# Kernel tuning notes

Hardware: AMD Instinct MI355X
Metric: run time of the kernel (lower is better)

## Reference

```python
import jax, jax.numpy as jnp
import numpy as np

DIM = 768
H = 12
D = DIM // H            # 64
SCALE = D ** -0.5
M = 64                  # landmarks for pnp heads
PINV_ITERS = 6
PNP_HEADS = 11          # heads 0..10 use Nystrom, head 11 uses softmax


def setup_inputs() -> dict:
    key = jax.random.key(0)
    ks = jax.random.split(key, 5)
    B, N = 4, 4096
    x = jax.random.normal(ks[0], (B, N, DIM), jnp.float32)
    qkv_w = jax.random.normal(ks[1], (3 * DIM, DIM), jnp.float32) * (DIM ** -0.5)
    qkv_b = jax.random.normal(ks[2], (3 * DIM,), jnp.float32) * 0.01
    proj_w = jax.random.normal(ks[3], (DIM, DIM), jnp.float32) * (DIM ** -0.5)
    proj_b = jax.random.normal(ks[4], (DIM,), jnp.float32) * 0.01
    return {"x": x, "qkv_w": qkv_w, "qkv_b": qkv_b, "proj_w": proj_w, "proj_b": proj_b}


def moore_penrose_iter_pinv(x, iters=PINV_ITERS):
    # x: [B, h, M, M]. Original torch code takes torch.max over the whole per-head
    # tensor (incl. batch), so normalize with a per-head scalar over axes (B, M).
    abs_x = jnp.abs(x)
    col_max = abs_x.sum(axis=-1, keepdims=True).max(axis=(0, 2, 3), keepdims=True)
    row_max = abs_x.sum(axis=-2, keepdims=True).max(axis=(0, 2, 3), keepdims=True)
    z = jnp.swapaxes(x, -1, -2) / (col_max * row_max)
    I = jnp.eye(x.shape[-1], dtype=x.dtype)
    for _ in range(iters):
        xz = x @ z
        z = 0.25 * (z @ (13.0 * I - xz @ (15.0 * I - xz @ (7.0 * I - xz))))
    return z


def reference(x, qkv_w, qkv_b, proj_w, proj_b):
    B, N, C = x.shape
    qkv = (x @ qkv_w.T + qkv_b).reshape(B, N, 3, H, D).transpose(2, 0, 3, 1, 4)  # [3,B,H,N,D]
    q, k, v = qkv[0] * SCALE, qkv[1], qkv[2]

    # ---- Nystrom (pnp) heads 0..PNP_HEADS-1, all with the same M -> vectorized ----
    qp, kp, vp = q[:, :PNP_HEADS], k[:, :PNP_HEADS], v[:, :PNP_HEADS]
    idxs = jnp.array([int(i * N / M) for i in range(M)], dtype=jnp.int32)
    q_m = qp[:, :, idxs, :]   # [B,h,M,D] landmark queries
    k_m = kp[:, :, idxs, :]   # [B,h,M,D] landmark keys

    SA = jnp.einsum('bhnd,bhmd->bhnm', qp, k_m)   # [B,h,N,M]
    SC = jnp.einsum('bhmd,bhnd->bhmn', q_m, kp)   # [B,h,M,N]
    SB = jnp.einsum('bhmd,bhld->bhml', q_m, k_m)  # [B,h,M,M]

    eA = jnp.exp(SA - SA.max(axis=-1, keepdims=True))
    sc_max = SC.max(axis=-1, keepdims=True)       # [B,h,M,1]
    eC = jnp.exp(SC - sc_max)
    eB = jnp.exp(jnp.clip(SB - sc_max, -88.0, None))

    v_aug = jnp.concatenate([vp, jnp.ones_like(vp[..., :1])], axis=-1)  # [B,h,N,D+1]
    pi = moore_penrose_iter_pinv(eB)
    prod = (eA @ pi) @ (eC @ v_aug)               # [B,h,N,D+1]
    out_p = prod[..., :-1] / jnp.maximum(prod[..., -1:], 1e-8)

    # ---- fallback softmax head(s) ----
    qs, ks_, vs = q[:, PNP_HEADS:], k[:, PNP_HEADS:], v[:, PNP_HEADS:]
    attn = jax.nn.softmax(jnp.einsum('bhnd,bhmd->bhnm', qs, ks_), axis=-1)
    out_s = attn @ vs

    ctx = jnp.concatenate([out_p, out_s], axis=1).transpose(0, 2, 1, 3).reshape(B, N, C)
    return ctx @ proj_w.T + proj_b
```

## Files before the change

### kernel.cpp

```cpp
#include <hip/hip_runtime.h>


typedef __attribute__((ext_vector_type(8))) short short8;
typedef __attribute__((ext_vector_type(4))) float f32x4;
typedef __attribute__((ext_vector_type(4))) unsigned short ushort4v;

static __device__ __forceinline__ unsigned short f2bf(float f) {
    union { float f; unsigned u; } x; x.f = f;
    unsigned r = x.u + 0x7fffu + ((x.u >> 16) & 1u);
    return (unsigned short)(r >> 16);
}

static __device__ __forceinline__ float b2f(unsigned short u) {
    union { unsigned u; float f; } t; t.u = (unsigned)u << 16; return t.f;
}

static __device__ __forceinline__ void bfsplit(float x, unsigned short& h, unsigned short& l) {
    unsigned short hh = f2bf(x);
    union { unsigned u; float f; } t; t.u = (unsigned)hh << 16;
    h = hh;
    l = f2bf(x - t.f);
}

__global__ __launch_bounds__(256) void preconv3(
    const float* __restrict__ a, const float* __restrict__ b,
    const float* __restrict__ c,
    unsigned short* __restrict__ ahi, unsigned short* __restrict__ alo,
    unsigned short* __restrict__ bhi, unsigned short* __restrict__ blo,
    unsigned short* __restrict__ chi, unsigned short* __restrict__ clo)
{
    const int nA = 3145728, nB = 442368, nC = 147456;
    const int total = nA + nB + nC;
    for (int i = blockIdx.x * 256 + threadIdx.x; i < total; i += gridDim.x * 256) {
        const float* src; unsigned short* hi; unsigned short* lo; int j;
        if (i < nA)           { src = a; hi = ahi; lo = alo; j = i; }
        else if (i < nA + nB) { src = b; hi = bhi; lo = blo; j = i - nA; }
        else                  { src = c; hi = chi; lo = clo; j = i - nA - nB; }
        float4 f = *(const float4*)(src + (size_t)j * 4);
        float vs[4] = {f.x, f.y, f.z, f.w};
        ushort4v h, l;
        #pragma unroll
        for (int t = 0; t < 4; ++t) {
            unsigned short hh, ll;
            bfsplit(vs[t], hh, ll);
            h[t] = hh; l[t] = ll;
        }
        *(ushort4v*)(hi + (size_t)j * 4) = h;
        *(ushort4v*)(lo + (size_t)j * 4) = l;
    }
}

__global__ __launch_bounds__(256, 2) void gemm_qk_mfma(
    const unsigned short* __restrict__ Xh, const unsigned short* __restrict__ Xl,
    const unsigned short* __restrict__ Wh, const unsigned short* __restrict__ Wl,
    const float* __restrict__ bias,
    unsigned short* __restrict__ qh, unsigned short* __restrict__ ql,
    unsigned short* __restrict__ kh, unsigned short* __restrict__ kl)
{
    __shared__ unsigned short Ah[4096], Al[4096], Bh[4096], Bl[4096];
    const int tid = threadIdx.x;
    const int bid = blockIdx.x;
    const int swz = (bid & 7) * 192 + (bid >> 3);
    const int brow = (swz / 12) << 7, bcol = (swz % 12) << 7;
    const int ln = tid & 63, wv = tid >> 6;
    const int wr = (wv >> 1) << 6, wc = (wv & 1) << 6;
    const int srow = tid >> 1, sc = (tid & 1) << 1;
    const size_t ag = (size_t)(brow + srow) * 768 + (sc << 3);
    const size_t bg = (size_t)(bcol + srow) * 768 + (sc << 3);
    const int fr = ln & 15, fc = ln >> 4;
    const int i0 = srow * 32 + (((sc + 0) ^ (srow & 3)) << 3);
    const int i1 = srow * 32 + (((sc + 1) ^ (srow & 3)) << 3);

    f32x4 acc[4][4] = {};
    for (int k0 = 0; k0 < 768; k0 += 32) {
        short8 xh0 = *(const short8*)(Xh + ag + k0);
        short8 xh1 = *(const short8*)(Xh + ag + k0 + 8);
        short8 xl0 = *(const short8*)(Xl + ag + k0);
        short8 xl1 = *(const short8*)(Xl + ag + k0 + 8);
        short8 wh0 = *(const short8*)(Wh + bg + k0);
        short8 wh1 = *(const short8*)(Wh + bg + k0 + 8);
        short8 wl0 = *(const short8*)(Wl + bg + k0);
        short8 wl1 = *(const short8*)(Wl + bg + k0 + 8);
        __syncthreads();
        *(short8*)&Ah[i0] = xh0; *(short8*)&Ah[i1] = xh1;
        *(short8*)&Al[i0] = xl0; *(short8*)&Al[i1] = xl1;
        *(short8*)&Bh[i0] = wh0; *(short8*)&Bh[i1] = wh1;
        *(short8*)&Bl[i0] = wl0; *(short8*)&Bl[i1] = wl1;
        __syncthreads();
        short8 ah[4], al[4], bh[4], bl[4];
        #pragma unroll
        for (int i = 0; i < 4; ++i) {
            int ar = wr + (i << 4) + fr;
            int aidx = ar * 32 + ((fc ^ (ar & 3)) << 3);
            ah[i] = *(short8*)&Ah[aidx];
            al[i] = *(short8*)&Al[aidx];
            int br2 = wc + (i << 4) + fr;
            int bidx = br2 * 32 + ((fc ^ (br2 & 3)) << 3);
            bh[i] = *(short8*)&Bh[bidx];
            bl[i] = *(short8*)&Bl[bidx];
        }
        #pragma unroll
        for (int i = 0; i < 4; ++i)
            #pragma unroll
            for (int j = 0; j < 4; ++j) {
                acc[i][j] = __builtin_amdgcn_mfma_f32_16x16x32_bf16(ah[i], bh[j], acc[i][j], 0, 0, 0);
                acc[i][j] = __builtin_amdgcn_mfma_f32_16x16x32_bf16(ah[i], bl[j], acc[i][j], 0, 0, 0);
                acc[i][j] = __builtin_amdgcn_mfma_f32_16x16x32_bf16(al[i], bh[j], acc[i][j], 0, 0, 0);
            }
    }
    const int fg = ln >> 4;
    #pragma unroll
    for (int j = 0; j < 4; ++j) {
        int c = bcol + wc + (j << 4) + fr;
        float bb = bias[c];
        int rem = c - (c >= 768 ? 768 : 0);
        int h = rem >> 6, d = rem & 63;
        #pragma unroll
        for (int i = 0; i < 4; ++i)
            #pragma unroll
            for (int r = 0; r < 4; ++r) {
                int row = brow + wr + (i << 4) + (fg << 2) + r;
                int b = row >> 12, n = row & 4095;
                float val = acc[i][j][r] + bb;
                size_t idx = (((size_t)(b * 12 + h) << 12) + n) * 64 + d;
                unsigned short hh, ll;
                if (c < 768) {
                    bfsplit(val * 0.125f, hh, ll);
                    qh[idx] = hh; ql[idx] = ll;
                } else {
                    bfsplit(val, hh, ll);
                    kh[idx] = hh; kl[idx] = ll;
                }
            }
    }
}

__global__ __launch_bounds__(256, 2) void gemm_v_mfma(
    const unsigned short* __restrict__ Xh, const unsigned short* __restrict__ Wh,
    const float* __restrict__ bias, unsigned short* __restrict__ vh)
{
    __shared__ unsigned short Ah[8192], Bh[8192];
    const int tid = threadIdx.x;
    const int bid = blockIdx.x;
    const int swz = (bid & 7) * 96 + (bid >> 3);
    const int brow = (swz / 6) << 7, bcol = 1536 + ((swz % 6) << 7);
    const int ln = tid & 63, wv = tid >> 6;
    const int wr = (wv >> 1) << 6, wc = (wv & 1) << 6;
    const int srow = tid >> 1;
    const int c0 = (tid & 1) << 2;
    const size_t ag = (size_t)(brow + srow) * 768;
    const size_t bg = (size_t)(bcol + srow) * 768;
    const int fr = ln & 15, fc = ln >> 4;

    f32x4 acc[4][4] = {};
    for (int k0 = 0; k0 < 768; k0 += 64) {
        short8 xa[4], wb[4];
        #pragma unroll
        for (int cc = 0; cc < 4; ++cc) {
            xa[cc] = *(const short8*)(Xh + ag + k0 + ((c0 + cc) << 3));
            wb[cc] = *(const short8*)(Wh + bg + k0 + ((c0 + cc) << 3));
        }
        __syncthreads();
        #pragma unroll
        for (int cc = 0; cc < 4; ++cc) {
            int dst = srow * 64 + (((c0 + cc) ^ (srow & 7)) << 3);
            *(short8*)&Ah[dst] = xa[cc];
            *(short8*)&Bh[dst] = wb[cc];
        }
        __syncthreads();
        #pragma unroll
        for (int ks = 0; ks < 2; ++ks) {
            const int kc = (ks << 2) + fc;
            short8 ah[4], bh[4];
            #pragma unroll
            for (int i = 0; i < 4; ++i) {
                int ar = wr + (i << 4) + fr;
                ah[i] = *(short8*)&Ah[ar * 64 + ((kc ^ (ar & 7)) << 3)];
                int br2 = wc + (i << 4) + fr;
                bh[i] = *(short8*)&Bh[br2 * 64 + ((kc ^ (br2 & 7)) << 3)];
            }
            #pragma unroll
            for (int i = 0; i < 4; ++i)
                #pragma unroll
                for (int j = 0; j < 4; ++j)
                    acc[i][j] = __builtin_amdgcn_mfma_f32_16x16x32_bf16(ah[i], bh[j], acc[i][j], 0, 0, 0);
        }
    }
    const int fg = ln >> 4;
    #pragma unroll
    for (int j = 0; j < 4; ++j) {
        int c = bcol + wc + (j << 4) + fr;
        float bb = bias[c];
        int rem = c - 1536;
        int h = rem >> 6, d = rem & 63;
        #pragma unroll
        for (int i = 0; i < 4; ++i)
            #pragma unroll
            for (int r = 0; r < 4; ++r) {
                int row = brow + wr + (i << 4) + (fg << 2) + r;
                int b = row >> 12, n = row & 4095;
                float val = acc[i][j][r] + bb;
                size_t idx = (((size_t)(b * 12 + h) << 12) + n) * 64 + d;
                vh[idx] = f2bf(val);
            }
    }
}

__global__ __launch_bounds__(256) void wflash(
    const unsigned short* __restrict__ qh, const unsigned short* __restrict__ ql,
    const unsigned short* __restrict__ khg, const unsigned short* __restrict__ klg,
    const unsigned short* __restrict__ vhg,
    float* __restrict__ wacc, float* __restrict__ wl, float* __restrict__ wm)
{
    int chunk = blockIdx.x;
    int bh = blockIdx.y;
    int b = bh / 11, h = bh - b * 11;
    size_t base = ((size_t)(b * 12 + h)) << 12;
    __shared__ unsigned short kh_s[64][72], kl_s[64][72];
    __shared__ unsigned short vth[64][72];
    __shared__ unsigned short ph[4][16][72];
    int tid = threadIdx.x;
    int wv = tid >> 6, ln = tid & 63;
    int rr = tid >> 2, dg = (tid & 3) << 4;
    const int arow = (wv << 4) + (ln & 15);
    const int ak0 = (ln >> 4) << 3;
    const int rg = (ln >> 4) << 2;
    short8 aqh0, aql0, aqh1, aql1;
    {
        size_t off = ((base + ((size_t)arow << 6)) << 6) + ak0;
        aqh0 = *(const short8*)(qh + off);
        aqh1 = *(const short8*)(qh + off + 32);
        aql0 = *(const short8*)(ql + off);
        aql1 = *(const short8*)(ql + off + 32);
    }
    f32x4 o_acc[4] = {};
    float mr[4] = {-1e30f, -1e30f, -1e30f, -1e30f};
    float lr[4] = {};
    for (int t = 0; t < 8; ++t) {
        int n0 = (chunk << 9) + (t << 6);
        __syncthreads();
        {
            size_t off = ((base + n0 + rr) << 6) + dg;
            *(short8*)&kh_s[rr][dg]     = *(const short8*)(khg + off);
            *(short8*)&kh_s[rr][dg + 8] = *(const short8*)(khg + off + 8);
            *(short8*)&kl_s[rr][dg]     = *(const short8*)(klg + off);
            *(short8*)&kl_s[rr][dg + 8] = *(const short8*)(klg + off + 8);
            short8 v0 = *(const short8*)(vhg + off);
            short8 v1 = *(const short8*)(vhg + off + 8);
            #pragma unroll
            for (int i = 0; i < 8; ++i) {
                vth[dg + i][rr]     = (unsigned short)v0[i];
                vth[dg + 8 + i][rr] = (unsigned short)v1[i];
            }
        }
        __syncthreads();
        f32x4 s_acc[4];
        #pragma unroll
        for (int jb = 0; jb < 4; ++jb) {
            f32x4 z = {};
            const int brow2 = (jb << 4) + (ln & 15);
            short8 bh0 = *(short8*)&kh_s[brow2][ak0];
            short8 bh1 = *(short8*)&kh_s[brow2][ak0 + 32];
            short8 bl0 = *(short8*)&kl_s[brow2][ak0];
            short8 bl1 = *(short8*)&kl_s[brow2][ak0 + 32];
            z = __builtin_amdgcn_mfma_f32_16x16x32_bf16(aqh0, bh0, z, 0, 0, 0);
            z = __builtin_amdgcn_mfma_f32_16x16x32_bf16(aqh0, bl0, z, 0, 0, 0);
            z = __builtin_amdgcn_mfma_f32_16x16x32_bf16(aql0, bh0, z, 0, 0, 0);
            z = __builtin_amdgcn_mfma_f32_16x16x32_bf16(aqh1, bh1, z, 0, 0, 0);
            z = __builtin_amdgcn_mfma_f32_16x16x32_bf16(aqh1, bl1, z, 0, 0, 0);
            z = __builtin_amdgcn_mfma_f32_16x16x32_bf16(aql1, bh1, z, 0, 0, 0);
            s_acc[jb] = z;
        }
        float mx[4];
        #pragma unroll
        for (int r = 0; r < 4; ++r)
            mx[r] = fmaxf(fmaxf(s_acc[0][r], s_acc[1][r]),
                          fmaxf(s_acc[2][r], s_acc[3][r]));
        #pragma unroll
        for (int off2 = 1; off2 < 16; off2 <<= 1)
            #pragma unroll
            for (int r = 0; r < 4; ++r)
                mx[r] = fmaxf(mx[r], __shfl_xor(mx[r], off2, 64));
        float fac[4];
        #pragma unroll
        for (int r = 0; r < 4; ++r) {
            float mn = fmaxf(mr[r], mx[r]);
            fac[r] = expf(mr[r] - mn);
            mr[r] = mn;
        }
        float rs[4] = {};
        #pragma unroll
        for (int jb = 0; jb < 4; ++jb)
            #pragma unroll
            for (int r = 0; r < 4; ++r) {
                float p = expf(s_acc[jb][r] - mr[r]);
                rs[r] += p;
                ph[wv][rg + r][(jb << 4) + (ln & 15)] = f2bf(p);
            }
        #pragma unroll
        for (int off2 = 1; off2 < 16; off2 <<= 1)
            #pragma unroll
            for (int r = 0; r < 4; ++r)
                rs[r] += __shfl_xor(rs[r], off2, 64);
        #pragma unroll
        for (int r = 0; r < 4; ++r) lr[r] = lr[r] * fac[r] + rs[r];
        #pragma unroll
        for (int jb = 0; jb < 4; ++jb)
            #pragma unroll
            for (int r = 0; r < 4; ++r)
                o_acc[jb][r] *= fac[r];
        short8 pah0 = *(short8*)&ph[wv][ln & 15][ak0];
        short8 pah1 = *(short8*)&ph[wv][ln & 15][ak0 + 32];
        #pragma unroll
        for (int jb = 0; jb < 4; ++jb) {
            const int brow2 = (jb << 4) + (ln & 15);
            short8 bv0 = *(short8*)&vth[brow2][ak0];
            short8 bv1 = *(short8*)&vth[brow2][ak0 + 32];
            f32x4 o = o_acc[jb];
            o = __builtin_amdgcn_mfma_f32_16x16x32_bf16(pah0, bv0, o, 0, 0, 0);
            o = __builtin_amdgcn_mfma_f32_16x16x32_bf16(pah1, bv1, o, 0, 0, 0);
            o_acc[jb] = o;
        }
    }
    int cidx = (bh << 3) + chunk;
    #pragma unroll
    for (int jb = 0; jb < 4; ++jb)
        #pragma unroll
        for (int r = 0; r < 4; ++r) {
            int row = (wv << 4) + rg + r, col = (jb << 4) + (ln & 15);
            wacc[((size_t)cidx << 12) + ((size_t)row << 6) + col] = o_acc[jb][r];
        }
    if ((ln & 15) == 0)
        #pragma unroll
        for (int r = 0; r < 4; ++r) {
            int row = (wv << 4) + rg + r;
            wl[cidx * 64 + row] = lr[r];
            wm[cidx * 64 + row] = mr[r];
        }
}

__global__ __launch_bounds__(256) void wmerge(
    const float* __restrict__ wacc, const float* __restrict__ wl,
    const float* __restrict__ wm,
    float* __restrict__ Wb, float* __restrict__ scm)
{
    int bh = blockIdx.x;
    int tid = threadIdx.x;
    __shared__ float fcs[8][64];
    if (tid < 64) {
        float mx = -1e30f;
        #pragma unroll
        for (int c = 0; c < 8; ++c)
            mx = fmaxf(mx, wm[((bh << 3) + c) * 64 + tid]);
        scm[(bh << 6) + tid] = mx;
        #pragma unroll
        for (int c = 0; c < 8; ++c)
            fcs[c][tid] = expf(wm[((bh << 3) + c) * 64 + tid] - mx);
    }
    __syncthreads();
    for (int e = tid; e < 4096; e += 256) {
        int m = e >> 6, j = e & 63;
        float s = 0.f;
        #pragma unroll
        for (int c = 0; c < 8; ++c)
            s += fcs[c][m] * wacc[((size_t)((bh << 3) + c) << 12) + e];
        Wb[(size_t)bh * 4160 + m * 65 + j] = s;
    }
    if (tid < 64) {
        float s = 0.f;
        #pragma unroll
        for (int c = 0; c < 8; ++c)
            s += fcs[c][tid] * wl[((bh << 3) + c) * 64 + tid];
        Wb[(size_t)bh * 4160 + tid * 65 + 64] = s;
    }
}

__global__ __launch_bounds__(256) void eb_kernel(
    const unsigned short* __restrict__ qh, const unsigned short* __restrict__ ql,
    const unsigned short* __restrict__ kh, const unsigned short* __restrict__ kl,
    const float* __restrict__ scm, float* __restrict__ eB)
{
    int bh = blockIdx.x;
    int b = bh / 11, h = bh - b * 11;
    size_t base = ((size_t)(b * 12 + h)) << 12;
    __shared__ float qm[64][65], km[64][65];
    int tid = threadIdx.x;
    for (int e = tid; e < 4096; e += 256) {
        int mm = e >> 6, d = e & 63;
        size_t off = ((base + ((size_t)mm << 6)) << 6) + d;
        qm[mm][d] = b2f(qh[off]) + b2f(ql[off]);
        km[mm][d] = b2f(kh[off]) + b2f(kl[off]);
    }
    __syncthreads();
    int m = tid >> 2, l0 = tid & 3;
    float smax = scm[(bh << 6) + m];
    for (int l = l0; l < 64; l += 4) {
        float s = 0.f;
        #pragma unroll
        for (int d = 0; d < 64; ++d) s += qm[m][d] * km[l][d];
        eB[((size_t)bh << 12) + (m << 6) + l] = expf(fmaxf(s - smax, -88.f));
    }
}

__global__ __launch_bounds__(256) void norms_kernel(
    const float* __restrict__ eB, float* __restrict__ denom)
{
    int h = blockIdx.x;
    int tid = threadIdx.x;
    int b = tid >> 6, idx = tid & 63;
    int bh = b * 11 + h;
    const float* E = eB + ((size_t)bh << 12);
    float rs = 0.f, cs = 0.f;
    #pragma unroll 4
    for (int l = 0; l < 64; ++l) rs += E[(idx << 6) + l];
    #pragma unroll 4
    for (int m = 0; m < 64; ++m) cs += E[(m << 6) + idx];
    __shared__ float r1[256], r2[256];
    r1[tid] = rs; r2[tid] = cs;
    __syncthreads();
    for (int s = 128; s > 0; s >>= 1) {
        if (tid < s) {
            r1[tid] = fmaxf(r1[tid], r1[tid + s]);
            r2[tid] = fmaxf(r2[tid], r2[tid + s]);
        }
        __syncthreads();
    }
    if (tid == 0) denom[h] = r1[0] * r2[0];
}

__device__ __forceinline__ void mm64x3(
    const unsigned short (&Ahi)[64][72], const unsigned short (&Alo)[64][72],
    const unsigned short (&BThi)[64][72], const unsigned short (&BTlo)[64][72],
    int wr, int wc, int fr, int fk, f32x4 (&acc)[2][2])
{
    #pragma unroll
    for (int ks = 0; ks < 2; ++ks) {
        const int kb = (ks << 5) + fk;
        short8 ah[2], al[2], bh[2], bl[2];
        #pragma unroll
        for (int i = 0; i < 2; ++i) {
            ah[i] = *(const short8*)&Ahi[wr + (i << 4) + fr][kb];
            al[i] = *(const short8*)&Alo[wr + (i << 4) + fr][kb];
            bh[i] = *(const short8*)&BThi[wc + (i << 4) + fr][kb];
            bl[i] = *(const short8*)&BTlo[wc + (i << 4) + fr][kb];
        }
        #pragma unroll
        for (int i = 0; i < 2; ++i)
            #pragma unroll
            for (int j = 0; j < 2; ++j) {
                acc[i][j] = __builtin_amdgcn_mfma_f32_16x16x32_bf16(ah[i], bh[j], acc[i][j], 0, 0, 0);
                acc[i][j] = __builtin_amdgcn_mfma_f32_16x16x32_bf16(ah[i], bl[j], acc[i][j], 0, 0, 0);
                acc[i][j] = __builtin_amdgcn_mfma_f32_16x16x32_bf16(al[i], bh[j], acc[i][j], 0, 0, 0);
            }
    }
}

__global__ __launch_bounds__(256) void pinv_kernel(
    const float* __restrict__ eB, const float* __restrict__ denom,
    float* __restrict__ pi_)
{
    __shared__ unsigned short Xh[64][72],  Xl[64][72];
    __shared__ unsigned short Zh[64][72],  Zl[64][72];
    __shared__ unsigned short ZTh[64][72], ZTl[64][72];
    __shared__ unsigned short Mh[64][72],  Ml[64][72];
    __shared__ unsigned short MTh[64][72], MTl[64][72];
    __shared__ unsigned short Th[64][72],  Tbl[64][72];
    __shared__ float Zf[64][68];
    int bh = blockIdx.x;
    int h = bh % 11;
    int tid = threadIdx.x;
    float dn = denom[h];
    const int ln = tid & 63, wv = tid >> 6;
    const int wr = (wv >> 1) << 5, wc = (wv & 1) << 5;
    const int fr = ln & 15, fk = (ln >> 4) << 3;
    const int rg = (ln >> 4) << 2;

    for (int e = tid; e < 4096; e += 256) {
        int m = e >> 6, l = e & 63;
        float xv = eB[((size_t)bh << 12) + e];
        unsigned short hh, ll;
        bfsplit(xv, hh, ll);
        Xh[m][l] = hh; Xl[m][l] = ll;
        float zv = xv / dn;
        Zf[l][m] = zv;
        bfsplit(zv, hh, ll);
        Zh[l][m] = hh; Zl[l][m] = ll;
        ZTh[m][l] = hh; ZTl[m][l] = ll;
    }
    __syncthreads();

    for (int it = 0; it < 6; ++it) {
        f32x4 mm1[2][2] = {};
        mm64x3(Xh, Xl, ZTh, ZTl, wr, wc, fr, fk, mm1);
        #pragma unroll
        for (int i = 0; i < 2; ++i)
            #pragma unroll
            for (int j = 0; j < 2; ++j)
                #pragma unroll
                for (int r = 0; r < 4; ++r) {
                    int row = wr + (i << 4) + rg + r, col = wc + (j << 4) + fr;
                    unsigned short hh, ll;
                    bfsplit(mm1[i][j][r], hh, ll);
                    Mh[row][col] = hh;  Ml[row][col] = ll;
                    MTh[col][row] = hh; MTl[col][row] = ll;
                }
        __syncthreads();
        f32x4 a2[2][2] = {};
        mm64x3(Mh, Ml, MTh, MTl, wr, wc, fr, fk, a2);
        #pragma unroll
        for (int i = 0; i < 2; ++i)
            #pragma unroll
            for (int j = 0; j < 2; ++j)
                #pragma unroll
                for (int r = 0; r < 4; ++r) {
                    int row = wr + (i << 4) + rg + r, col = wc + (j << 4) + fr;
                    float val = 7.f * mm1[i][j][r] - a2[i][j][r];
                    unsigned short hh, ll;
                    bfsplit(val, hh, ll);
                    Th[col][row] = hh; Tbl[col][row] = ll;
                }
        __syncthreads();
        f32x4 a3[2][2] = {};
        mm64x3(Mh, Ml, Th, Tbl, wr, wc, fr, fk, a3);
        __syncthreads();
        #pragma unroll
        for (int i = 0; i < 2; ++i)
            #pragma unroll
            for (int j = 0; j < 2; ++j)
                #pragma unroll
                for (int r = 0; r < 4; ++r) {
                    int row = wr + (i << 4) + rg + r, col = wc + (j << 4) + fr;
                    float val = 15.f * mm1[i][j][r] - a3[i][j][r];
                    unsigned short hh, ll;
                    bfsplit(val, hh, ll);
                    Th[col][row] = hh; Tbl[col][row] = ll;
                }
        __syncthreads();
        f32x4 a4[2][2] = {};
        mm64x3(Zh, Zl, Th, Tbl, wr, wc, fr, fk, a4);
        float zn[2][2][4];
        #pragma unroll
        for (int i = 0; i < 2; ++i)
            #pragma unroll
            for (int j = 0; j < 2; ++j)
                #pragma unroll
                for (int r = 0; r < 4; ++r) {
                    int row = wr + (i << 4) + rg + r, col = wc + (j << 4) + fr;
                    zn[i][j][r] = 0.25f * (13.f * Zf[row][col] - a4[i][j][r]);
                }
        __syncthreads();
        #pragma unroll
        for (int i = 0; i < 2; ++i)
            #pragma unroll
            for (int j = 0; j < 2; ++j)
                #pragma unroll
                for (int r = 0; r < 4; ++r) {
                    int row = wr + (i << 4) + rg + r, col = wc + (j << 4) + fr;
                    float val = zn[i][j][r];
                    Zf[row][col] = val;
                    unsigned short hh, ll;
                    bfsplit(val, hh, ll);
                    Zh[row][col] = hh;  Zl[row][col] = ll;
                    ZTh[col][row] = hh; ZTl[col][row] = ll;
                }
        __syncthreads();
    }
    for (int e = tid; e < 4096; e += 256)
        pi_[((size_t)bh << 12) + e] = Zf[e >> 6][e & 63];
}

__global__ __launch_bounds__(256) void pw_kernel(
    const float* __restrict__ pi_, const float* __restrict__ Wb,
    float* __restrict__ Tb)
{
    int bh = blockIdx.x;
    __shared__ float P[64][65];
    __shared__ float Wl[64][66];
    int tid = threadIdx.x;
    for (int e = tid; e < 4096; e += 256)
        P[e >> 6][e & 63] = pi_[((size_t)bh << 12) + e];
    for (int e = tid; e < 64 * 65; e += 256) {
        int l = e / 65, j = e - l * 65;
        Wl[l][j] = Wb[(size_t)bh * 4160 + e];
    }
    __syncthreads();
    int m = tid & 63, g = tid >> 6;
    #pragma unroll
    for (int t = 0; t < 17; ++t) {
        int j = g + (t << 2);
        if (j > 64) break;
        float s = 0.f;
        #pragma unroll
        for (int l = 0; l < 64; ++l) s += P[m][l] * Wl[l][j];
        Tb[(size_t)((bh << 6) + m) * 65 + j] = s;
    }
}

__global__ __launch_bounds__(256) void outp_kernel(
    const unsigned short* __restrict__ qh, const unsigned short* __restrict__ ql,
    const unsigned short* __restrict__ khg, const unsigned short* __restrict__ klg,
    const float* __restrict__ Tb, unsigned short* __restrict__ ctxh)
{
    int bh = blockIdx.y;
    int b = bh / 11, h = bh - b * 11;
    int n0 = blockIdx.x << 6;
    size_t base = ((size_t)(b * 12 + h)) << 12;
    __shared__ unsigned short kmh[64][72], kml[64][72];
    __shared__ unsigned short tth[64][72], ttl[64][72];
    __shared__ unsigned short ph[4][16][72];
    __shared__ float t64[64];
    int tid = threadIdx.x;
    int wv = tid >> 6, ln = tid & 63;
    int rr = tid >> 2, dg = (tid & 3) << 4;
    const int arow = (wv << 4) + (ln & 15);
    const int ak0 = (ln >> 4) << 3;
    const int rg = (ln >> 4) << 2;
    {
        size_t off = ((base + ((size_t)rr << 6)) << 6) + dg;
        *(short8*)&kmh[rr][dg]     = *(const short8*)(khg + off);
        *(short8*)&kmh[rr][dg + 8] = *(const short8*)(khg + off + 8);
        *(short8*)&kml[rr][dg]     = *(const short8*)(klg + off);
        *(short8*)&kml[rr][dg + 8] = *(const short8*)(klg + off + 8);
    }
    for (int e = tid; e < 4096; e += 256) {
        int m = e >> 6, j = e & 63;
        float tv = Tb[(size_t)((bh << 6) + m) * 65 + j];
        unsigned short hh, ll;
        bfsplit(tv, hh, ll);
        tth[j][m] = hh; ttl[j][m] = ll;
    }
    if (tid < 64) t64[tid] = Tb[(size_t)((bh << 6) + tid) * 65 + 64];
    short8 aqh0, aql0, aqh1, aql1;
    {
        size_t off = ((base + n0 + arow) << 6) + ak0;
        aqh0 = *(const short8*)(qh + off);
        aqh1 = *(const short8*)(qh + off + 32);
        aql0 = *(const short8*)(ql + off);
        aql1 = *(const short8*)(ql + off + 32);
    }
    __syncthreads();
    f32x4 s_acc[4];
    #pragma unroll
    for (int jb = 0; jb < 4; ++jb) {
        f32x4 z = {};
        const int brow2 = (jb << 4) + (ln & 15);
        short8 bh0 = *(short8*)&kmh[brow2][ak0];
        short8 bh1 = *(short8*)&kmh[brow2][ak0 + 32];
        short8 bl0 = *(short8*)&kml[brow2][ak0];
        short8 bl1 = *(short8*)&kml[brow2][ak0 + 32];
        z = __builtin_amdgcn_mfma_f32_16x16x32_bf16(aqh0, bh0, z, 0, 0, 0);
        z = __builtin_amdgcn_mfma_f32_16x16x32_bf16(aqh0, bl0, z, 0, 0, 0);
        z = __builtin_amdgcn_mfma_f32_16x16x32_bf16(aql0, bh0, z, 0, 0, 0);
        z = __builtin_amdgcn_mfma_f32_16x16x32_bf16(aqh1, bh1, z, 0, 0, 0);
        z = __builtin_amdgcn_mfma_f32_16x16x32_bf16(aqh1, bl1, z, 0, 0, 0);
        z = __builtin_amdgcn_mfma_f32_16x16x32_bf16(aql1, bh1, z, 0, 0, 0);
        s_acc[jb] = z;
    }
    float mx[4];
    #pragma unroll
    for (int r = 0; r < 4; ++r)
        mx[r] = fmaxf(fmaxf(s_acc[0][r], s_acc[1][r]),
                      fmaxf(s_acc[2][r], s_acc[3][r]));
    #pragma unroll
    for (int off2 = 1; off2 < 16; off2 <<= 1)
        #pragma unroll
        for (int r = 0; r < 4; ++r)
            mx[r] = fmaxf(mx[r], __shfl_xor(mx[r], off2, 64));
    float den[4] = {};
    #pragma unroll
    for (int jb = 0; jb < 4; ++jb) {
        float tj = t64[(jb << 4) + (ln & 15)];
        #pragma unroll
        for (int r = 0; r < 4; ++r) {
            float p = expf(s_acc[jb][r] - mx[r]);
            den[r] += p * tj;
            ph[wv][rg + r][(jb << 4) + (ln & 15)] = f2bf(p);
        }
    }
    #pragma unroll
    for (int off2 = 1; off2 < 16; off2 <<= 1)
        #pragma unroll
        for (int r = 0; r < 4; ++r)
            den[r] += __shfl_xor(den[r], off2, 64);
    short8 pah0 = *(short8*)&ph[wv][ln & 15][ak0];
    short8 pah1 = *(short8*)&ph[wv][ln & 15][ak0 + 32];
    f32x4 o_acc[4] = {};
    #pragma unroll
    for (int jb = 0; jb < 4; ++jb) {
        const int brow2 = (jb << 4) + (ln & 15);
        short8 bth0 = *(short8*)&tth[brow2][ak0];
        short8 bth1 = *(short8*)&tth[brow2][ak0 + 32];
        short8 btl0 = *(short8*)&ttl[brow2][ak0];
        short8 btl1 = *(short8*)&ttl[brow2][ak0 + 32];
        f32x4 o = o_acc[jb];
        o = __builtin_amdgcn_mfma_f32_16x16x32_bf16(pah0, bth0, o, 0, 0, 0);
        o = __builtin_amdgcn_mfma_f32_16x16x32_bf16(pah0, btl0, o, 0, 0, 0);
        o = __builtin_amdgcn_mfma_f32_16x16x32_bf16(pah1, bth1, o, 0, 0, 0);
        o = __builtin_amdgcn_mfma_f32_16x16x32_bf16(pah1, btl1, o, 0, 0, 0);
        o_acc[jb] = o;
    }
    float inv[4];
    #pragma unroll
    for (int r = 0; r < 4; ++r) inv[r] = 1.0f / fmaxf(den[r], 1e-8f);
    #pragma unroll
    for (int jb = 0; jb < 4; ++jb)
        #pragma unroll
        for (int r = 0; r < 4; ++r) {
            int row = n0 + (wv << 4) + rg + r;
            int col = (jb << 4) + (ln & 15);
            ctxh[((size_t)b * 4096 + row) * 768 + h * 64 + col] =
                f2bf(o_acc[jb][r] * inv[r]);
        }
}

__global__ __launch_bounds__(256) void flash_part(
    const unsigned short* __restrict__ qhg, const unsigned short* __restrict__ khg,
    const unsigned short* __restrict__ vhg,
    float* __restrict__ pacc, float* __restrict__ pm, float* __restrict__ pl)
{
    int bx = blockIdx.x, cy = blockIdx.y, b = blockIdx.z;
    int n0 = bx << 6;
    size_t base = ((size_t)(b * 12 + 11)) << 12;
    __shared__ unsigned short qs[64][72];
    __shared__ unsigned short ks[64][72];
    __shared__ unsigned short vts[64][72];
    __shared__ unsigned short ps[4][16][72];
    int tid = threadIdx.x;
    int wv = tid >> 6, ln = tid & 63;
    int rr = tid >> 2, dg = (tid & 3) << 4;
    {
        size_t off = ((base + n0 + rr) << 6) + dg;
        *(short8*)&qs[rr][dg]     = *(const short8*)(qhg + off);
        *(short8*)&qs[rr][dg + 8] = *(const short8*)(qhg + off + 8);
    }
    __syncthreads();
    const int arow = (wv << 4) + (ln & 15);
    const int ak0 = (ln >> 4) << 3;
    const int rg = (ln >> 4) << 2;
    short8 aq0 = *(short8*)&qs[arow][ak0];
    short8 aq1 = *(short8*)&qs[arow][ak0 + 32];
    f32x4 o_acc[4] = {};
    float mr[4] = {-1e30f, -1e30f, -1e30f, -1e30f};
    float lr[4] = {};
    for (int t = 0; t < 16; ++t) {
        int m0 = (cy << 10) + (t << 6);
        __syncthreads();
        {
            size_t off = ((base + m0 + rr) << 6) + dg;
            *(short8*)&ks[rr][dg]     = *(const short8*)(khg + off);
            *(short8*)&ks[rr][dg + 8] = *(const short8*)(khg + off + 8);
            short8 v0 = *(const short8*)(vhg + off);
            short8 v1 = *(const short8*)(vhg + off + 8);
            #pragma unroll
            for (int i = 0; i < 8; ++i) {
                vts[dg + i][rr]     = (unsigned short)v0[i];
                vts[dg + 8 + i][rr] = (unsigned short)v1[i];
            }
        }
        __syncthreads();
        f32x4 s_acc[4];
        #pragma unroll
        for (int jb = 0; jb < 4; ++jb) {
            f32x4 z = {};
            short8 bk0 = *(short8*)&ks[(jb << 4) + (ln & 15)][ak0];
            short8 bk1 = *(short8*)&ks[(jb << 4) + (ln & 15)][ak0 + 32];
            z = __builtin_amdgcn_mfma_f32_16x16x32_bf16(aq0, bk0, z, 0, 0, 0);
            z = __builtin_amdgcn_mfma_f32_16x16x32_bf16(aq1, bk1, z, 0, 0, 0);
            s_acc[jb] = z;
        }
        float mx[4];
        #pragma unroll
        for (int r = 0; r < 4; ++r)
            mx[r] = fmaxf(fmaxf(s_acc[0][r], s_acc[1][r]),
                          fmaxf(s_acc[2][r], s_acc[3][r]));
        #pragma unroll
        for (int off2 = 1; off2 < 16; off2 <<= 1)
            #pragma unroll
            for (int r = 0; r < 4; ++r)
                mx[r] = fmaxf(mx[r], __shfl_xor(mx[r], off2, 64));
        float fac[4];
        #pragma unroll
        for (int r = 0; r < 4; ++r) {
            float mn = fmaxf(mr[r], mx[r]);
            fac[r] = expf(mr[r] - mn);
            mr[r] = mn;
        }
        float rs[4] = {};
        #pragma unroll
        for (int jb = 0; jb < 4; ++jb)
            #pragma unroll
            for (int r = 0; r < 4; ++r) {
                float p = expf(s_acc[jb][r] - mr[r]);
                rs[r] += p;
                ps[wv][rg + r][(jb << 4) + (ln & 15)] = f2bf(p);
            }
        #pragma unroll
        for (int off2 = 1; off2 < 16; off2 <<= 1)
            #pragma unroll
            for (int r = 0; r < 4; ++r)
                rs[r] += __shfl_xor(rs[r], off2, 64);
        #pragma unroll
        for (int r = 0; r < 4; ++r) lr[r] = lr[r] * fac[r] + rs[r];
        #pragma unroll
        for (int jb = 0; jb < 4; ++jb)
            #pragma unroll
            for (int r = 0; r < 4; ++r)
                o_acc[jb][r] *= fac[r];
        short8 pa0 = *(short8*)&ps[wv][ln & 15][ak0];
        short8 pa1 = *(short8*)&ps[wv][ln & 15][ak0 + 32];
        #pragma unroll
        for (int jb = 0; jb < 4; ++jb) {
            short8 bv0 = *(short8*)&vts[(jb << 4) + (ln & 15)][ak0];
            short8 bv1 = *(short8*)&vts[(jb << 4) + (ln & 15)][ak0 + 32];
            f32x4 z = o_acc[jb];
            z = __builtin_amdgcn_mfma_f32_16x16x32_bf16(pa0, bv0, z, 0, 0, 0);
            z = __builtin_amdgcn_mfma_f32_16x16x32_bf16(pa1, bv1, z, 0, 0, 0);
            o_acc[jb] = z;
        }
    }
    int slot = (b * 4 + cy) * 64 + bx;
    #pragma unroll
    for (int jb = 0; jb < 4; ++jb)
        #pragma unroll
        for (int r = 0; r < 4; ++r) {
            int row = (wv << 4) + rg + r, col = (jb << 4) + (ln & 15);
            pacc[(size_t)slot * 4096 + (size_t)row * 64 + col] = o_acc[jb][r];
        }
    if ((ln & 15) == 0)
        #pragma unroll
        for (int r = 0; r < 4; ++r) {
            int row = (wv << 4) + rg + r;
            pm[(size_t)slot * 64 + row] = mr[r];
            pl[(size_t)slot * 64 + row] = lr[r];
        }
}

__global__ __launch_bounds__(256) void flash_merge(
    const float* __restrict__ pacc, const float* __restrict__ pm,
    const float* __restrict__ pl, unsigned short* __restrict__ ctxh)
{
    int bx = blockIdx.x, b = blockIdx.y;
    int tid = threadIdx.x, r = tid & 63, g = tid >> 6;
    float mc[4], mt = -1e30f;
    #pragma unroll
    for (int c = 0; c < 4; ++c) {
        mc[c] = pm[(size_t)((b * 4 + c) * 64 + bx) * 64 + r];
        mt = fmaxf(mt, mc[c]);
    }
    float fac[4], lt = 0.f;
    #pragma unroll
    for (int c = 0; c < 4; ++c) {
        fac[c] = expf(mc[c] - mt);
        lt += fac[c] * pl[(size_t)((b * 4 + c) * 64 + bx) * 64 + r];
    }
    float inv = 1.0f / lt;
    size_t obase = ((size_t)b * 4096 + (size_t)((bx << 6) + r)) * 768 + 11 * 64 + (g << 4);
    #pragma unroll
    for (int i = 0; i < 16; ++i) {
        float s = 0.f;
        #pragma unroll
        for (int c = 0; c < 4; ++c)
            s += fac[c] * pacc[(size_t)((b * 4 + c) * 64 + bx) * 4096 + (size_t)r * 64 + (g << 4) + i];
        ctxh[obase + i] = f2bf(s * inv);
    }
}

__global__ __launch_bounds__(256, 2) void gemm_proj_mfma(
    const unsigned short* __restrict__ Xh, const unsigned short* __restrict__ Wh,
    const float* __restrict__ bias, float* __restrict__ out)
{
    __shared__ unsigned short Ah[8192], Bh[8192];
    const int tid = threadIdx.x;
    const int bid = blockIdx.x;
    const int swz = (bid & 7) * 96 + (bid >> 3);
    const int brow = (swz / 6) << 7, bcol = (swz % 6) << 7;
    const int ln = tid & 63, wv = tid >> 6;
    const int wr = (wv >> 1) << 6, wc = (wv & 1) << 6;
    const int srow = tid >> 1;
    const int c0 = (tid & 1) << 2;
    const size_t ag = (size_t)(brow + srow) * 768;
    const size_t bg = (size_t)(bcol + srow) * 768;
    const int fr = ln & 15, fc = ln >> 4;

    f32x4 acc[4][4] = {};
    for (int k0 = 0; k0 < 768; k0 += 64) {
        short8 xa[4], wb[4];
        #pragma unroll
        for (int cc = 0; cc < 4; ++cc) {
            xa[cc] = *(const short8*)(Xh + ag + k0 + ((c0 + cc) << 3));
            wb[cc] = *(const short8*)(Wh + bg + k0 + ((c0 + cc) << 3));
        }
        __syncthreads();
        #pragma unroll
        for (int cc = 0; cc < 4; ++cc) {
            int dst = srow * 64 + (((c0 + cc) ^ (srow & 7)) << 3);
            *(short8*)&Ah[dst] = xa[cc];
            *(short8*)&Bh[dst] = wb[cc];
        }
        __syncthreads();
        #pragma unroll
        for (int ks = 0; ks < 2; ++ks) {
            const int kc = (ks << 2) + fc;
            short8 ah[4], bh[4];
            #pragma unroll
            for (int i = 0; i < 4; ++i) {
                int ar = wr + (i << 4) + fr;
                ah[i] = *(short8*)&Ah[ar * 64 + ((kc ^ (ar & 7)) << 3)];
                int br2 = wc + (i << 4) + fr;
                bh[i] = *(short8*)&Bh[br2 * 64 + ((kc ^ (br2 & 7)) << 3)];
            }
            #pragma unroll
            for (int i = 0; i < 4; ++i)
                #pragma unroll
                for (int j = 0; j < 4; ++j)
                    acc[i][j] = __builtin_amdgcn_mfma_f32_16x16x32_bf16(ah[i], bh[j], acc[i][j], 0, 0, 0);
        }
    }
    const int fg = ln >> 4;
    #pragma unroll
    for (int j = 0; j < 4; ++j) {
        int c = bcol + wc + (j << 4) + fr;
        float bb = bias[c];
        #pragma unroll
        for (int i = 0; i < 4; ++i)
            #pragma unroll
            for (int r = 0; r < 4; ++r) {
                int row = brow + wr + (i << 4) + (fg << 2) + r;
                out[(size_t)row * 768 + c] = acc[i][j][r] + bb;
            }
    }
}

extern "C" void kernel_launch(void* const* d_in, const int* in_sizes, int n_in,
                              void* d_out, int out_size, void* d_ws, size_t ws_size,
                              hipStream_t stream)
{
    const float* x      = (const float*)d_in[0];
    const float* qkv_w  = (const float*)d_in[1];
    const float* qkv_b  = (const float*)d_in[2];
    const float* proj_w = (const float*)d_in[3];
    const float* proj_b = (const float*)d_in[4];
    float* out = (float*)d_out;

    const size_t QKV = (size_t)4 * 12 * 4096 * 64;
    unsigned short* qh = (unsigned short*)d_ws;
    unsigned short* ql = qh + QKV;
    unsigned short* kh = ql + QKV;
    unsigned short* kl = kh + QKV;
    unsigned short* vh = kl + QKV;
    unsigned short* ctxh = vh + QKV;
    float* scm  = (float*)(ctxh + QKV);
    float* eB   = scm + 4096;
    float* den  = eB + 44 * 4096;
    float* pi_  = den + 64;
    float* Wb   = pi_ + 44 * 4096;
    float* Tb   = Wb + 44 * 4160;
    unsigned short* Whi  = (unsigned short*)(Tb + 44 * 4160);
    unsigned short* Wlo  = Whi + (size_t)2304 * 768;
    unsigned short* Pwhi = Wlo + (size_t)2304 * 768;
    unsigned short* Pwlo = Pwhi + (size_t)768 * 768;

    unsigned short* Xhi = (unsigned short*)out;
    unsigned short* Xlo = Xhi + QKV;
    float* wacc = out;
    float* wl   = wacc + 1441792;
    float* wm   = wl + 22528;
    float* fpacc = out;
    float* fpm   = fpacc + 4194304;
    float* fpl   = fpm + 65536;

    preconv3<<<2048, 256, 0, stream>>>(x, qkv_w, proj_w,
                                       Xhi, Xlo, Whi, Wlo, Pwhi, Pwlo);
    gemm_qk_mfma<<<1536, 256, 0, stream>>>(Xhi, Xlo, Whi, Wlo, qkv_b,
                                           qh, ql, kh, kl);
    gemm_v_mfma<<<768, 256, 0, stream>>>(Xhi, Whi, qkv_b, vh);
    wflash<<<dim3(8, 44), 256, 0, stream>>>(qh, ql, kh, kl, vh, wacc, wl, wm);
    wmerge<<<44, 256, 0, stream>>>(wacc, wl, wm, Wb, scm);
    eb_kernel<<<44, 256, 0, stream>>>(qh, ql, kh, kl, scm, eB);
    norms_kernel<<<11, 256, 0, stream>>>(eB, den);
    pinv_kernel<<<44, 256, 0, stream>>>(eB, den, pi_);
    pw_kernel<<<44, 256, 0, stream>>>(pi_, Wb, Tb);
    outp_kernel<<<dim3(64, 44), 256, 0, stream>>>(qh, ql, kh, kl, Tb, ctxh);
    flash_part<<<dim3(64, 4, 4), 256, 0, stream>>>(qh, kh, vh, fpacc, fpm, fpl);
    flash_merge<<<dim3(64, 4), 256, 0, stream>>>(fpacc, fpm, fpl, ctxh);
    gemm_proj_mfma<<<768, 256, 0, stream>>>(ctxh, Pwhi, proj_b, out);
}
```

Baseline: 436.9 us.

## Merge independent kernels into combined launches to overlap softmax head with Nystrom stages

Fuses the QK and V projection GEMMs into one launch that branches on block index. It also merges the Nystrom landmark flash pass with the softmax-head partial flash into one attention launch, wmerge with eB computation, and outp with flash_merge. The goal is fewer launches and less tail idle time, letting independent work fill the GPU concurrently. The scratch buffers for the two flash paths now sit at separate offsets so they can coexist. The cost is heterogeneous blocks with differing shared-memory and register needs within a single kernel.

```diff
diff --git a/kernel.cpp b/kernel.cpp
--- a/kernel.cpp
+++ b/kernel.cpp
@@ -50,172 +50,168 @@
     }
 }
 
-__global__ __launch_bounds__(256, 2) void gemm_qk_mfma(
+__global__ __launch_bounds__(256, 2) void gemm_qkv2(
     const unsigned short* __restrict__ Xh, const unsigned short* __restrict__ Xl,
     const unsigned short* __restrict__ Wh, const unsigned short* __restrict__ Wl,
     const float* __restrict__ bias,
     unsigned short* __restrict__ qh, unsigned short* __restrict__ ql,
-    unsigned short* __restrict__ kh, unsigned short* __restrict__ kl)
-{
-    __shared__ unsigned short Ah[4096], Al[4096], Bh[4096], Bl[4096];
+    unsigned short* __restrict__ kh, unsigned short* __restrict__ kl,
+    unsigned short* __restrict__ vh)
+{
+    __shared__ unsigned short smem[16384];
     const int tid = threadIdx.x;
-    const int bid = blockIdx.x;
-    const int swz = (bid & 7) * 192 + (bid >> 3);
-    const int brow = (swz / 12) << 7, bcol = (swz % 12) << 7;
     const int ln = tid & 63, wv = tid >> 6;
     const int wr = (wv >> 1) << 6, wc = (wv & 1) << 6;
-    const int srow = tid >> 1, sc = (tid & 1) << 1;
-    const size_t ag = (size_t)(brow + srow) * 768 + (sc << 3);
-    const size_t bg = (size_t)(bcol + srow) * 768 + (sc << 3);
     const int fr = ln & 15, fc = ln >> 4;
-    const int i0 = srow * 32 + (((sc + 0) ^ (srow & 3)) << 3);
-    const int i1 = srow * 32 + (((sc + 1) ^ (srow & 3)) << 3);
-
-    f32x4 acc[4][4] = {};
-    for (int k0 = 0; k0 < 768; k0 += 32) {
-        short8 xh0 = *(const short8*)(Xh + ag + k0);
-        short8 xh1 = *(const short8*)(Xh + ag + k0 + 8);
-        short8 xl0 = *(const short8*)(Xl + ag + k0);
-        short8 xl1 = *(const short8*)(Xl + ag + k0 + 8);
-        short8 wh0 = *(const short8*)(Wh + bg + k0);
-        short8 wh1 = *(const short8*)(Wh + bg + k0 + 8);
-        short8 wl0 = *(const short8*)(Wl + bg + k0);
-        short8 wl1 = *(const short8*)(Wl + bg + k0 + 8);
-        __syncthreads();
-        *(short8*)&Ah[i0] = xh0; *(short8*)&Ah[i1] = xh1;
-        *(short8*)&Al[i0] = xl0; *(short8*)&Al[i1] = xl1;
-        *(short8*)&Bh[i0] = wh0; *(short8*)&Bh[i1] = wh1;
-        *(short8*)&Bl[i0] = wl0; *(short8*)&Bl[i1] = wl1;
-        __syncthreads();
-        short8 ah[4], al[4], bh[4], bl[4];
-        #pragma unroll
-        for (int i = 0; i < 4; ++i) {
-            int ar = wr + (i << 4) + fr;
-            int aidx = ar * 32 + ((fc ^ (ar & 3)) << 3);
-            ah[i] = *(short8*)&Ah[aidx];
-            al[i] = *(short8*)&Al[aidx];
-            int br2 = wc + (i << 4) + fr;
-            int bidx = br2 * 32 + ((fc ^ (br2 & 3)) << 3);
-            bh[i] = *(short8*)&Bh[bidx];
-            bl[i] = *(short8*)&Bl[bidx];
-        }
-        #pragma unroll
-        for (int i = 0; i < 4; ++i)
-            #pragma unroll
-            for (int j = 0; j < 4; ++j) {
-                acc[i][j] = __builtin_amdgcn_mfma_f32_16x16x32_bf16(ah[i], bh[j], acc[i][j], 0, 0, 0);
-                acc[i][j] = __builtin_amdgcn_mfma_f32_16x16x32_bf16(ah[i], bl[j], acc[i][j], 0, 0, 0);
-                acc[i][j] = __builtin_amdgcn_mfma_f32_16x16x32_bf16(al[i], bh[j], acc[i][j], 0, 0, 0);
-            }
-    }
     const int fg = ln >> 4;
-    #pragma unroll
-    for (int j = 0; j < 4; ++j) {
-        int c = bcol + wc + (j << 4) + fr;
-        float bb = bias[c];
-        int rem = c - (c >= 768 ? 768 : 0);
-        int h = rem >> 6, d = rem & 63;
-        #pragma unroll
-        for (int i = 0; i < 4; ++i)
-            #pragma unroll
-            for (int r = 0; r < 4; ++r) {
-                int row = brow + wr + (i << 4) + (fg << 2) + r;
-                int b = row >> 12, n = row & 4095;
-                float val = acc[i][j][r] + bb;
-                size_t idx = (((size_t)(b * 12 + h) << 12) + n) * 64 + d;
-                unsigned short hh, ll;
-                if (c < 768) {
-                    bfsplit(val * 0.125f, hh, ll);
-                    qh[idx] = hh; ql[idx] = ll;
-                } else {
-                    bfsplit(val, hh, ll);
-                    kh[idx] = hh; kl[idx] = ll;
-                }
-            }
-    }
-}
-
-__global__ __launch_bounds__(256, 2) void gemm_v_mfma(
-    const unsigned short* __restrict__ Xh, const unsigned short* __restrict__ Wh,
-    const float* __restrict__ bias, unsigned short* __restrict__ vh)
-{
-    __shared__ unsigned short Ah[8192], Bh[8192];
-    const int tid = threadIdx.x;
-    const int bid = blockIdx.x;
-    const int swz = (bid & 7) * 96 + (bid >> 3);
-    const int brow = (swz / 6) << 7, bcol = 1536 + ((swz % 6) << 7);
-    const int ln = tid & 63, wv = tid >> 6;
-    const int wr = (wv >> 1) << 6, wc = (wv & 1) << 6;
-    const int srow = tid >> 1;
-    const int c0 = (tid & 1) << 2;
-    const size_t ag = (size_t)(brow + srow) * 768;
-    const size_t bg = (size_t)(bcol + srow) * 768;
-    const int fr = ln & 15, fc = ln >> 4;
-
-    f32x4 acc[4][4] = {};
-    for (int k0 = 0; k0 < 768; k0 += 64) {
-        short8 xa[4], wb[4];
-        #pragma unroll
-        for (int cc = 0; cc < 4; ++cc) {
-            xa[cc] = *(const short8*)(Xh + ag + k0 + ((c0 + cc) << 3));
-            wb[cc] = *(const short8*)(Wh + bg + k0 + ((c0 + cc) << 3));
-        }
-        __syncthreads();
-        #pragma unroll
-        for (int cc = 0; cc < 4; ++cc) {
-            int dst = srow * 64 + (((c0 + cc) ^ (srow & 7)) << 3);
-            *(short8*)&Ah[dst] = xa[cc];
-            *(short8*)&Bh[dst] = wb[cc];
-        }
-        __syncthreads();
-        #pragma unroll
-        for (int ks = 0; ks < 2; ++ks) {
-            const int kc = (ks << 2) + fc;
-            short8 ah[4], bh[4];
+
+    if (blockIdx.x < 1536) {
+        unsigned short* Ah = smem;
+        unsigned short* Al = smem + 4096;
+        unsigned short* Bh = smem + 8192;
+        unsigned short* Bl = smem + 12288;
+        const int bid = blockIdx.x;
+        const int swz = (bid & 7) * 192 + (bid >> 3);
+        const int brow = (swz / 12) << 7, bcol = (swz % 12) << 7;
+        const int srow = tid >> 1, sc = (tid & 1) << 1;
+        const size_t ag = (size_t)(brow + srow) * 768 + (sc << 3);
+        const size_t bg = (size_t)(bcol + srow) * 768 + (sc << 3);
+        const int i0 = srow * 32 + (((sc + 0) ^ (srow & 3)) << 3);
+        const int i1 = srow * 32 + (((sc + 1) ^ (srow & 3)) << 3);
+
+        f32x4 acc[4][4] = {};
+        for (int k0 = 0; k0 < 768; k0 += 32) {
+            short8 xh0 = *(const short8*)(Xh + ag + k0);
+            short8 xh1 = *(const short8*)(Xh + ag + k0 + 8);
+            short8 xl0 = *(const short8*)(Xl + ag + k0);
+            short8 xl1 = *(const short8*)(Xl + ag + k0 + 8);
+            short8 wh0 = *(const short8*)(Wh + bg + k0);
+            short8 wh1 = *(const short8*)(Wh + bg + k0 + 8);
+            short8 wl0 = *(const short8*)(Wl + bg + k0);
+            short8 wl1 = *(const short8*)(Wl + bg + k0 + 8);
+            __syncthreads();
+            *(short8*)&Ah[i0] = xh0; *(short8*)&Ah[i1] = xh1;
+            *(short8*)&Al[i0] = xl0; *(short8*)&Al[i1] = xl1;
+            *(short8*)&Bh[i0] = wh0; *(short8*)&Bh[i1] = wh1;
+            *(short8*)&Bl[i0] = wl0; *(short8*)&Bl[i1] = wl1;
+            __syncthreads();
+            short8 ah[4], al[4], bh[4], bl[4];
             #pragma unroll
             for (int i = 0; i < 4; ++i) {
                 int ar = wr + (i << 4) + fr;
-                ah[i] = *(short8*)&Ah[ar * 64 + ((kc ^ (ar & 7)) << 3)];
+                int aidx = ar * 32 + ((fc ^ (ar & 3)) << 3);
+                ah[i] = *(short8*)&Ah[aidx];
+                al[i] = *(short8*)&Al[aidx];
                 int br2 = wc + (i << 4) + fr;
-                bh[i] = *(short8*)&Bh[br2 * 64 + ((kc ^ (br2 & 7)) << 3)];
+                int bidx = br2 * 32 + ((fc ^ (br2 & 3)) << 3);
+                bh[i] = *(short8*)&Bh[bidx];
+                bl[i] = *(short8*)&Bl[bidx];
             }
             #pragma unroll
             for (int i = 0; i < 4; ++i)
                 #pragma unroll
-                for (int j = 0; j < 4; ++j)
+                for (int j = 0; j < 4; ++j) {
                     acc[i][j] = __builtin_amdgcn_mfma_f32_16x16x32_bf16(ah[i], bh[j], acc[i][j], 0, 0, 0);
-        }
-    }
-    const int fg = ln >> 4;
-    #pragma unroll
-    for (int j = 0; j < 4; ++j) {
-        int c = bcol + wc + (j << 4) + fr;
-        float bb = bias[c];
-        int rem = c - 1536;
-        int h = rem >> 6, d = rem & 63;
-        #pragma unroll
-        for (int i = 0; i < 4; ++i)
-            #pragma unroll
-            for (int r = 0; r < 4; ++r) {
-                int row = brow + wr + (i << 4) + (fg << 2) + r;
-                int b = row >> 12, n = row & 4095;
-                float val = acc[i][j][r] + bb;
-                size_t idx = (((size_t)(b * 12 + h) << 12) + n) * 64 + d;
-                vh[idx] = f2bf(val);
-            }
-    }
-}
-
-__global__ __launch_bounds__(256) void wflash(
+                    acc[i][j] = __builtin_amdgcn_mfma_f32_16x16x32_bf16(ah[i], bl[j], acc[i][j], 0, 0, 0);
+                    acc[i][j] = __builtin_amdgcn_mfma_f32_16x16x32_bf16(al[i], bh[j], acc[i][j], 0, 0, 0);
+                }
+        }
+        #pragma unroll
+        for (int j = 0; j < 4; ++j) {
+            int c = bcol + wc + (j << 4) + fr;
+            float bb = bias[c];
+            int rem = c - (c >= 768 ? 768 : 0);
+            int h = rem >> 6, d = rem & 63;
+            #pragma unroll
+            for (int i = 0; i < 4; ++i)
+                #pragma unroll
+                for (int r = 0; r < 4; ++r) {
+                    int row = brow + wr + (i << 4) + (fg << 2) + r;
+                    int b = row >> 12, n = row & 4095;
+                    float val = acc[i][j][r] + bb;
+                    size_t idx = (((size_t)(b * 12 + h) << 12) + n) * 64 + d;
+                    unsigned short hh, ll;
+                    if (c < 768) {
+                        bfsplit(val * 0.125f, hh, ll);
+                        qh[idx] = hh; ql[idx] = ll;
+                    } else {
+                        bfsplit(val, hh, ll);
+                        kh[idx] = hh; kl[idx] = ll;
+                    }
+                }
+        }
+    } else {
+        unsigned short* Av = smem;
+        unsigned short* Bv = smem + 8192;
+        const int bid = blockIdx.x - 1536;
+        const int swz = (bid & 7) * 96 + (bid >> 3);
+        const int brow = (swz / 6) << 7, bcol = 1536 + ((swz % 6) << 7);
+        const int srow = tid >> 1;
+        const int c0 = (tid & 1) << 2;
+        const size_t ag = (size_t)(brow + srow) * 768;
+        const size_t bg = (size_t)(bcol + srow) * 768;
+
+        f32x4 acc[4][4] = {};
+        for (int k0 = 0; k0 < 768; k0 += 64) {
+            short8 xa[4], wb[4];
+            #pragma unroll
+            for (int cc = 0; cc < 4; ++cc) {
+                xa[cc] = *(const short8*)(Xh + ag + k0 + ((c0 + cc) << 3));
+                wb[cc] = *(const short8*)(Wh + bg + k0 + ((c0 + cc) << 3));
+            }
+            __syncthreads();
+            #pragma unroll
+            for (int cc = 0; cc < 4; ++cc) {
+                int dst = srow * 64 + (((c0 + cc) ^ (srow & 7)) << 3);
+                *(short8*)&Av[dst] = xa[cc];
+                *(short8*)&Bv[dst] = wb[cc];
+            }
+            __syncthreads();
+            #pragma unroll
+            for (int ks = 0; ks < 2; ++ks) {
+                const int kc = (ks << 2) + fc;
+                short8 ah[4], bh[4];
+                #pragma unroll
+                for (int i = 0; i < 4; ++i) {
+                    int ar = wr + (i << 4) + fr;
+                    ah[i] = *(short8*)&Av[ar * 64 + ((kc ^ (ar & 7)) << 3)];
+                    int br2 = wc + (i << 4) + fr;
+                    bh[i] = *(short8*)&Bv[br2 * 64 + ((kc ^ (br2 & 7)) << 3)];
+                }
+                #pragma unroll
+                for (int i = 0; i < 4; ++i)
+                    #pragma unroll
+                    for (int j = 0; j < 4; ++j)
+                        acc[i][j] = __builtin_amdgcn_mfma_f32_16x16x32_bf16(ah[i], bh[j], acc[i][j], 0, 0, 0);
+            }
+        }
+        #pragma unroll
+        for (int j = 0; j < 4; ++j) {
+            int c = bcol + wc + (j << 4) + fr;
+            float bb = bias[c];
+            int rem = c - 1536;
+            int h = rem >> 6, d = rem & 63;
+            #pragma unroll
+            for (int i = 0; i < 4; ++i)
+                #pragma unroll
+                for (int r = 0; r < 4; ++r) {
+                    int row = brow + wr + (i << 4) + (fg << 2) + r;
+                    int b = row >> 12, n = row & 4095;
+                    float val = acc[i][j][r] + bb;
+                    size_t idx = (((size_t)(b * 12 + h) << 12) + n) * 64 + d;
+                    vh[idx] = f2bf(val);
+                }
+        }
+    }
+}
+
+__global__ __launch_bounds__(256) void attn_mega(
     const unsigned short* __restrict__ qh, const unsigned short* __restrict__ ql,
     const unsigned short* __restrict__ khg, const unsigned short* __restrict__ klg,
     const unsigned short* __restrict__ vhg,
-    float* __restrict__ wacc, float* __restrict__ wl, float* __restrict__ wm)
-{
-    int chunk = blockIdx.x;
-    int bh = blockIdx.y;
-    int b = bh / 11, h = bh - b * 11;
-    size_t base = ((size_t)(b * 12 + h)) << 12;
+    float* __restrict__ wacc, float* __restrict__ wl, float* __restrict__ wm,
+    float* __restrict__ pacc, float* __restrict__ pm, float* __restrict__ pl)
+{
     __shared__ unsigned short kh_s[64][72], kl_s[64][72];
     __shared__ unsigned short vth[64][72];
     __shared__ unsigned short ph[4][16][72];
@@ -225,175 +221,283 @@
     const int arow = (wv << 4) + (ln & 15);
     const int ak0 = (ln >> 4) << 3;
     const int rg = (ln >> 4) << 2;
-    short8 aqh0, aql0, aqh1, aql1;
-    {
-        size_t off = ((base + ((size_t)arow << 6)) << 6) + ak0;
-        aqh0 = *(const short8*)(qh + off);
-        aqh1 = *(const short8*)(qh + off + 32);
-        aql0 = *(const short8*)(ql + off);
-        aql1 = *(const short8*)(ql + off + 32);
-    }
-    f32x4 o_acc[4] = {};
-    float mr[4] = {-1e30f, -1e30f, -1e30f, -1e30f};
-    float lr[4] = {};
-    for (int t = 0; t < 8; ++t) {
-        int n0 = (chunk << 9) + (t << 6);
-        __syncthreads();
+
+    if (blockIdx.x < 1024) {
+        int fbid = blockIdx.x;
+        int bx = fbid & 63, cy = (fbid >> 6) & 3, b = fbid >> 8;
+        int n0 = bx << 6;
+        size_t base = ((size_t)(b * 12 + 11)) << 12;
         {
             size_t off = ((base + n0 + rr) << 6) + dg;
-            *(short8*)&kh_s[rr][dg]     = *(const short8*)(khg + off);
-            *(short8*)&kh_s[rr][dg + 8] = *(const short8*)(khg + off + 8);
-            *(short8*)&kl_s[rr][dg]     = *(const short8*)(klg + off);
-            *(short8*)&kl_s[rr][dg + 8] = *(const short8*)(klg + off + 8);
-            short8 v0 = *(const short8*)(vhg + off);
-            short8 v1 = *(const short8*)(vhg + off + 8);
-            #pragma unroll
-            for (int i = 0; i < 8; ++i) {
-                vth[dg + i][rr]     = (unsigned short)v0[i];
-                vth[dg + 8 + i][rr] = (unsigned short)v1[i];
-            }
-        }
-        __syncthreads();
-        f32x4 s_acc[4];
-        #pragma unroll
-        for (int jb = 0; jb < 4; ++jb) {
-            f32x4 z = {};
-            const int brow2 = (jb << 4) + (ln & 15);
-            short8 bh0 = *(short8*)&kh_s[brow2][ak0];
-            short8 bh1 = *(short8*)&kh_s[brow2][ak0 + 32];
-            short8 bl0 = *(short8*)&kl_s[brow2][ak0];
-            short8 bl1 = *(short8*)&kl_s[brow2][ak0 + 32];
-            z = __builtin_amdgcn_mfma_f32_16x16x32_bf16(aqh0, bh0, z, 0, 0, 0);
-            z = __builtin_amdgcn_mfma_f32_16x16x32_bf16(aqh0, bl0, z, 0, 0, 0);
-            z = __builtin_amdgcn_mfma_f32_16x16x32_bf16(aql0, bh0, z, 0, 0, 0);
-            z = __builtin_amdgcn_mfma_f32_16x16x32_bf16(aqh1, bh1, z, 0, 0, 0);
-            z = __builtin_amdgcn_mfma_f32_16x16x32_bf16(aqh1, bl1, z, 0, 0, 0);
-            z = __builtin_amdgcn_mfma_f32_16x16x32_bf16(aql1, bh1, z, 0, 0, 0);
-            s_acc[jb] = z;
-        }
-        float mx[4];
-        #pragma unroll
-        for (int r = 0; r < 4; ++r)
-            mx[r] = fmaxf(fmaxf(s_acc[0][r], s_acc[1][r]),
-                          fmaxf(s_acc[2][r], s_acc[3][r]));
-        #pragma unroll
-        for (int off2 = 1; off2 < 16; off2 <<= 1)
+            *(short8*)&kh_s[rr][dg]     = *(const short8*)(qh + off);
+            *(short8*)&kh_s[rr][dg + 8] = *(const short8*)(qh + off + 8);
+        }
+        __syncthreads();
+        short8 aq0 = *(short8*)&kh_s[arow][ak0];
+        short8 aq1 = *(short8*)&kh_s[arow][ak0 + 32];
+        f32x4 o_acc[4] = {};
+        float mr[4] = {-1e30f, -1e30f, -1e30f, -1e30f};
+        float lr[4] = {};
+        for (int t = 0; t < 16; ++t) {
+            int m0 = (cy << 10) + (t << 6);
+            __syncthreads();
+            {
+                size_t off = ((base + m0 + rr) << 6) + dg;
+                *(short8*)&kl_s[rr][dg]     = *(const short8*)(khg + off);
+                *(short8*)&kl_s[rr][dg + 8] = *(const short8*)(khg + off + 8);
+                short8 v0 = *(const short8*)(vhg + off);
+                short8 v1 = *(const short8*)(vhg + off + 8);
+                #pragma unroll
+                for (int i = 0; i < 8; ++i) {
+                    vth[dg + i][rr]     = (unsigned short)v0[i];
+                    vth[dg + 8 + i][rr] = (unsigned short)v1[i];
+                }
+            }
+            __syncthreads();
+            f32x4 s_acc[4];
+            #pragma unroll
+            for (int jb = 0; jb < 4; ++jb) {
+                f32x4 z = {};
+                short8 bk0 = *(short8*)&kl_s[(jb << 4) + (ln & 15)][ak0];
+                short8 bk1 = *(short8*)&kl_s[(jb << 4) + (ln & 15)][ak0 + 32];
+                z = __builtin_amdgcn_mfma_f32_16x16x32_bf16(aq0, bk0, z, 0, 0, 0);
+                z = __builtin_amdgcn_mfma_f32_16x16x32_bf16(aq1, bk1, z, 0, 0, 0);
+                s_acc[jb] = z;
+            }
+            float mx[4];
             #pragma unroll
             for (int r = 0; r < 4; ++r)
-                mx[r] = fmaxf(mx[r], __shfl_xor(mx[r], off2, 64));
-        float fac[4];
-        #pragma unroll
-        for (int r = 0; r < 4; ++r) {
-            float mn = fmaxf(mr[r], mx[r]);
-            fac[r] = expf(mr[r] - mn);
-            mr[r] = mn;
-        }
-        float rs[4] = {};
+                mx[r] = fmaxf(fmaxf(s_acc[0][r], s_acc[1][r]),
+                              fmaxf(s_acc[2][r], s_acc[3][r]));
+            #pragma unroll
+            for (int off2 = 1; off2 < 16; off2 <<= 1)
+                #pragma unroll
+                for (int r = 0; r < 4; ++r)
+                    mx[r] = fmaxf(mx[r], __shfl_xor(mx[r], off2, 64));
+            float fac[4];
+            #pragma unroll
+            for (int r = 0; r < 4; ++r) {
+                float mn = fmaxf(mr[r], mx[r]);
+                fac[r] = expf(mr[r] - mn);
+                mr[r] = mn;
+            }
+            float rs[4] = {};
+            #pragma unroll
+            for (int jb = 0; jb < 4; ++jb)
+                #pragma unroll
+                for (int r = 0; r < 4; ++r) {
+                    float p = expf(s_acc[jb][r] - mr[r]);
+                    rs[r] += p;
+                    ph[wv][rg + r][(jb << 4) + (ln & 15)] = f2bf(p);
+                }
+            #pragma unroll
+            for (int off2 = 1; off2 < 16; off2 <<= 1)
+                #pragma unroll
+                for (int r = 0; r < 4; ++r)
+                    rs[r] += __shfl_xor(rs[r], off2, 64);
+            #pragma unroll
+            for (int r = 0; r < 4; ++r) lr[r] = lr[r] * fac[r] + rs[r];
+            #pragma unroll
+            for (int jb = 0; jb < 4; ++jb)
+                #pragma unroll
+                for (int r = 0; r < 4; ++r)
+                    o_acc[jb][r] *= fac[r];
+            short8 pa0 = *(short8*)&ph[wv][ln & 15][ak0];
+            short8 pa1 = *(short8*)&ph[wv][ln & 15][ak0 + 32];
+            #pragma unroll
+            for (int jb = 0; jb < 4; ++jb) {
+                short8 bv0 = *(short8*)&vth[(jb << 4) + (ln & 15)][ak0];
+                short8 bv1 = *(short8*)&vth[(jb << 4) + (ln & 15)][ak0 + 32];
+                f32x4 z = o_acc[jb];
+                z = __builtin_amdgcn_mfma_f32_16x16x32_bf16(pa0, bv0, z, 0, 0, 0);
+                z = __builtin_amdgcn_mfma_f32_16x16x32_bf16(pa1, bv1, z, 0, 0, 0);
+                o_acc[jb] = z;
+            }
+        }
+        int slot = (b * 4 + cy) * 64 + bx;
         #pragma unroll
         for (int jb = 0; jb < 4; ++jb)
             #pragma unroll
             for (int r = 0; r < 4; ++r) {
-                float p = expf(s_acc[jb][r] - mr[r]);
-                rs[r] += p;
-                ph[wv][rg + r][(jb << 4) + (ln & 15)] = f2bf(p);
-            }
-        #pragma unroll
-        for (int off2 = 1; off2 < 16; off2 <<= 1)
+                int row = (wv << 4) + rg + r, col = (jb << 4) + (ln & 15);
+                pacc[(size_t)slot * 4096 + (size_t)row * 64 + col] = o_acc[jb][r];
+            }
+        if ((ln & 15) == 0)
+            #pragma unroll
+            for (int r = 0; r < 4; ++r) {
+                int row = (wv << 4) + rg + r;
+                pm[(size_t)slot * 64 + row] = mr[r];
+                pl[(size_t)slot * 64 + row] = lr[r];
+            }
+    } else {
+        int wbid = blockIdx.x - 1024;
+        int chunk = wbid & 7;
+        int bh = wbid >> 3;
+        int b = bh / 11, h = bh - b * 11;
+        size_t base = ((size_t)(b * 12 + h)) << 12;
+        short8 aqh0, aql0, aqh1, aql1;
+        {
+            size_t off = ((base + ((size_t)arow << 6)) << 6) + ak0;
+            aqh0 = *(const short8*)(qh + off);
+            aqh1 = *(const short8*)(qh + off + 32);
+            aql0 = *(const short8*)(ql + off);
+            aql1 = *(const short8*)(ql + off + 32);
+        }
+        f32x4 o_acc[4] = {};
+        float mr[4] = {-1e30f, -1e30f, -1e30f, -1e30f};
+        float lr[4] = {};
+        for (int t = 0; t < 8; ++t) {
+            int n0 = (chunk << 9) + (t << 6);
+            __syncthreads();
+            {
+                size_t off = ((base + n0 + rr) << 6) + dg;
+                *(short8*)&kh_s[rr][dg]     = *(const short8*)(khg + off);
+                *(short8*)&kh_s[rr][dg + 8] = *(const short8*)(khg + off + 8);
+                *(short8*)&kl_s[rr][dg]     = *(const short8*)(klg + off);
+                *(short8*)&kl_s[rr][dg + 8] = *(const short8*)(klg + off + 8);
+                short8 v0 = *(const short8*)(vhg + off);
+                short8 v1 = *(const short8*)(vhg + off + 8);
+                #pragma unroll
+                for (int i = 0; i < 8; ++i) {
+                    vth[dg + i][rr]     = (unsigned short)v0[i];
+                    vth[dg + 8 + i][rr] = (unsigned short)v1[i];
+                }
+            }
+            __syncthreads();
+            f32x4 s_acc[4];
+            #pragma unroll
+            for (int jb = 0; jb < 4; ++jb) {
+                f32x4 z = {};
+                const int brow2 = (jb << 4) + (ln & 15);
+                short8 bh0 = *(short8*)&kh_s[brow2][ak0];
+                short8 bh1 = *(short8*)&kh_s[brow2][ak0 + 32];
+                short8 bl0 = *(short8*)&kl_s[brow2][ak0];
+                short8 bl1 = *(short8*)&kl_s[brow2][ak0 + 32];
+                z = __builtin_amdgcn_mfma_f32_16x16x32_bf16(aqh0, bh0, z, 0, 0, 0);
+                z = __builtin_amdgcn_mfma_f32_16x16x32_bf16(aqh0, bl0, z, 0, 0, 0);
+                z = __builtin_amdgcn_mfma_f32_16x16x32_bf16(aql0, bh0, z, 0, 0, 0);
+                z = __builtin_amdgcn_mfma_f32_16x16x32_bf16(aqh1, bh1, z, 0, 0, 0);
+                z = __builtin_amdgcn_mfma_f32_16x16x32_bf16(aqh1, bl1, z, 0, 0, 0);
+                z = __builtin_amdgcn_mfma_f32_16x16x32_bf16(aql1, bh1, z, 0, 0, 0);
+                s_acc[jb] = z;
+            }
+            float mx[4];
             #pragma unroll
             for (int r = 0; r < 4; ++r)
-                rs[r] += __shfl_xor(rs[r], off2, 64);
-        #pragma unroll
-        for (int r = 0; r < 4; ++r) lr[r] = lr[r] * fac[r] + rs[r];
+                mx[r] = fmaxf(fmaxf(s_acc[0][r], s_acc[1][r]),
+                              fmaxf(s_acc[2][r], s_acc[3][r]));
+            #pragma unroll
+            for (int off2 = 1; off2 < 16; off2 <<= 1)
+                #pragma unroll
+                for (int r = 0; r < 4; ++r)
+                    mx[r] = fmaxf(mx[r], __shfl_xor(mx[r], off2, 64));
+            float fac[4];
+            #pragma unroll
+            for (int r = 0; r < 4; ++r) {
+                float mn = fmaxf(mr[r], mx[r]);
+                fac[r] = expf(mr[r] - mn);
+                mr[r] = mn;
+            }
+            float rs[4] = {};
+            #pragma unroll
+            for (int jb = 0; jb < 4; ++jb)
+                #pragma unroll
+                for (int r = 0; r < 4; ++r) {
+                    float p = expf(s_acc[jb][r] - mr[r]);
+                    rs[r] += p;
+                    ph[wv][rg + r][(jb << 4) + (ln & 15)] = f2bf(p);
+                }
+            #pragma unroll
+            for (int off2 = 1; off2 < 16; off2 <<= 1)
+                #pragma unroll
+                for (int r = 0; r < 4; ++r)
+                    rs[r] += __shfl_xor(rs[r], off2, 64);
+            #pragma unroll
+            for (int r = 0; r < 4; ++r) lr[r] = lr[r] * fac[r] + rs[r];
+            #pragma unroll
+            for (int jb = 0; jb < 4; ++jb)
+                #pragma unroll
+                for (int r = 0; r < 4; ++r)
+                    o_acc[jb][r] *= fac[r];
+            short8 pah0 = *(short8*)&ph[wv][ln & 15][ak0];
+            short8 pah1 = *(short8*)&ph[wv][ln & 15][ak0 + 32];
+            #pragma unroll
+            for (int jb = 0; jb < 4; ++jb) {
+                const int brow2 = (jb << 4) + (ln & 15);
+                short8 bv0 = *(short8*)&vth[brow2][ak0];
+                short8 bv1 = *(short8*)&vth[brow2][ak0 + 32];
+                f32x4 o = o_acc[jb];
+                o = __builtin_amdgcn_mfma_f32_16x16x32_bf16(pah0, bv0, o, 0, 0, 0);
+                o = __builtin_amdgcn_mfma_f32_16x16x32_bf16(pah1, bv1, o, 0, 0, 0);
+                o_acc[jb] = o;
+            }
+        }
+        int cidx = (bh << 3) + chunk;
         #pragma unroll
         for (int jb = 0; jb < 4; ++jb)
             #pragma unroll
-            for (int r = 0; r < 4; ++r)
-                o_acc[jb][r] *= fac[r];
-        short8 pah0 = *(short8*)&ph[wv][ln & 15][ak0];
-        short8 pah1 = *(short8*)&ph[wv][ln & 15][ak0 + 32];
-        #pragma unroll
-        for (int jb = 0; jb < 4; ++jb) {
-            const int brow2 = (jb << 4) + (ln & 15);
-            short8 bv0 = *(short8*)&vth[brow2][ak0];
-            short8 bv1 = *(short8*)&vth[brow2][ak0 + 32];
-            f32x4 o = o_acc[jb];
-            o = __builtin_amdgcn_mfma_f32_16x16x32_bf16(pah0, bv0, o, 0, 0, 0);
-            o = __builtin_amdgcn_mfma_f32_16x16x32_bf16(pah1, bv1, o, 0, 0, 0);
-            o_acc[jb] = o;
-        }
-    }
-    int cidx = (bh << 3) + chunk;
-    #pragma unroll
-    for (int jb = 0; jb < 4; ++jb)
-        #pragma unroll
-        for (int r = 0; r < 4; ++r) {
-            int row = (wv << 4) + rg + r, col = (jb << 4) + (ln & 15);
-            wacc[((size_t)cidx << 12) + ((size_t)row << 6) + col] = o_acc[jb][r];
-        }
-    if ((ln & 15) == 0)
-        #pragma unroll
-        for (int r = 0; r < 4; ++r) {
-            int row = (wv << 4) + rg + r;
-            wl[cidx * 64 + row] = lr[r];
-            wm[cidx * 64 + row] = mr[r];
-        }
-}
-
-__global__ __launch_bounds__(256) void wmerge(
+            for (int r = 0; r < 4; ++r) {
+                int row = (wv << 4) + rg + r, col = (jb << 4) + (ln & 15);
+                wacc[((size_t)cidx << 12) + ((size_t)row << 6) + col] = o_acc[jb][r];
+            }
+        if ((ln & 15) == 0)
+            #pragma unroll
+            for (int r = 0; r < 4; ++r) {
+                int row = (wv << 4) + rg + r;
+                wl[cidx * 64 + row] = lr[r];
+                wm[cidx * 64 + row] = mr[r];
+            }
+    }
+}
+
+__global__ __launch_bounds__(256) void wmerge_eb(
     const float* __restrict__ wacc, const float* __restrict__ wl,
     const float* __restrict__ wm,
-    float* __restrict__ Wb, float* __restrict__ scm)
-{
-    int bh = blockIdx.x;
-    int tid = threadIdx.x;
-    __shared__ float fcs[8][64];
-    if (tid < 64) {
-        float mx = -1e30f;
-        #pragma unroll
-        for (int c = 0; c < 8; ++c)
-            mx = fmaxf(mx, wm[((bh << 3) + c) * 64 + tid]);
-        scm[(bh << 6) + tid] = mx;
-        #pragma unroll
-        for (int c = 0; c < 8; ++c)
-            fcs[c][tid] = expf(wm[((bh << 3) + c) * 64 + tid] - mx);
-    }
-    __syncthreads();
-    for (int e = tid; e < 4096; e += 256) {
-        int m = e >> 6, j = e & 63;
-        float s = 0.f;
-        #pragma unroll
-        for (int c = 0; c < 8; ++c)
-            s += fcs[c][m] * wacc[((size_t)((bh << 3) + c) << 12) + e];
-        Wb[(size_t)bh * 4160 + m * 65 + j] = s;
-    }
-    if (tid < 64) {
-        float s = 0.f;
-        #pragma unroll
-        for (int c = 0; c < 8; ++c)
-            s += fcs[c][tid] * wl[((bh << 3) + c) * 64 + tid];
-        Wb[(size_t)bh * 4160 + tid * 65 + 64] = s;
-    }
-}
-
-__global__ __launch_bounds__(256) void eb_kernel(
     const unsigned short* __restrict__ qh, const unsigned short* __restrict__ ql,
     const unsigned short* __restrict__ kh, const unsigned short* __restrict__ kl,
-    const float* __restrict__ scm, float* __restrict__ eB)
+    float* __restrict__ Wb, float* __restrict__ eB)
 {
     int bh = blockIdx.x;
     int b = bh / 11, h = bh - b * 11;
     size_t base = ((size_t)(b * 12 + h)) << 12;
+    int tid = threadIdx.x;
+    __shared__ float fcs[8][64];
+    __shared__ float scms[64];
     __shared__ float qm[64][65], km[64][65];
-    int tid = threadIdx.x;
     for (int e = tid; e < 4096; e += 256) {
         int mm = e >> 6, d = e & 63;
         size_t off = ((base + ((size_t)mm << 6)) << 6) + d;
         qm[mm][d] = b2f(qh[off]) + b2f(ql[off]);
         km[mm][d] = b2f(kh[off]) + b2f(kl[off]);
     }
+    if (tid < 64) {
+        float mx = -1e30f;
+        #pragma unroll
+        for (int c = 0; c < 8; ++c)
+            mx = fmaxf(mx, wm[((bh << 3) + c) * 64 + tid]);
+        scms[tid] = mx;
+        #pragma unroll
+        for (int c = 0; c < 8; ++c)
+            fcs[c][tid] = expf(wm[((bh << 3) + c) * 64 + tid] - mx);
+    }
     __syncthreads();
+    for (int e = tid; e < 4096; e += 256) {
+        int m = e >> 6, j = e & 63;
+        float s = 0.f;
+        #pragma unroll
+        for (int c = 0; c < 8; ++c)
+            s += fcs[c][m] * wacc[((size_t)((bh << 3) + c) << 12) + e];
+        Wb[(size_t)bh * 4160 + m * 65 + j] = s;
+    }
+    if (tid < 64) {
+        float s = 0.f;
+        #pragma unroll
+        for (int c = 0; c < 8; ++c)
+            s += fcs[c][tid] * wl[((bh << 3) + c) * 64 + tid];
+        Wb[(size_t)bh * 4160 + tid * 65 + 64] = s;
+    }
     int m = tid >> 2, l0 = tid & 3;
-    float smax = scm[(bh << 6) + m];
+    float smax = scms[m];
     for (int l = l0; l < 64; l += 4) {
         float s = 0.f;
         #pragma unroll
@@ -596,176 +700,69 @@
     }
 }
 
-__global__ __launch_bounds__(256) void outp_kernel(
+__global__ __launch_bounds__(256) void outp_merge(
     const unsigned short* __restrict__ qh, const unsigned short* __restrict__ ql,
     const unsigned short* __restrict__ khg, const unsigned short* __restrict__ klg,
-    const float* __restrict__ Tb, unsigned short* __restrict__ ctxh)
-{
-    int bh = blockIdx.y;
-    int b = bh / 11, h = bh - b * 11;
-    int n0 = blockIdx.x << 6;
-    size_t base = ((size_t)(b * 12 + h)) << 12;
-    __shared__ unsigned short kmh[64][72], kml[64][72];
-    __shared__ unsigned short tth[64][72], ttl[64][72];
-    __shared__ unsigned short ph[4][16][72];
-    __shared__ float t64[64];
+    const float* __restrict__ Tb,
+    const float* __restrict__ pacc, const float* __restrict__ pm,
+    const float* __restrict__ pl,
+    unsigned short* __restrict__ ctxh)
+{
     int tid = threadIdx.x;
-    int wv = tid >> 6, ln = tid & 63;
-    int rr = tid >> 2, dg = (tid & 3) << 4;
-    const int arow = (wv << 4) + (ln & 15);
-    const int ak0 = (ln >> 4) << 3;
-    const int rg = (ln >> 4) << 2;
-    {
-        size_t off = ((base + ((size_t)rr << 6)) << 6) + dg;
-        *(short8*)&kmh[rr][dg]     = *(const short8*)(khg + off);
-        *(short8*)&kmh[rr][dg + 8] = *(const short8*)(khg + off + 8);
-        *(short8*)&kml[rr][dg]     = *(const short8*)(klg + off);
-        *(short8*)&kml[rr][dg + 8] = *(const short8*)(klg + off + 8);
-    }
-    for (int e = tid; e < 4096; e += 256) {
-        int m = e >> 6, j = e & 63;
-        float tv = Tb[(size_t)((bh << 6) + m) * 65 + j];
-        unsigned short hh, ll;
-        bfsplit(tv, hh, ll);
-        tth[j][m] = hh; ttl[j][m] = ll;
-    }
-    if (tid < 64) t64[tid] = Tb[(size_t)((bh << 6) + tid) * 65 + 64];
-    short8 aqh0, aql0, aqh1, aql1;
-    {
-        size_t off = ((base + n0 + arow) << 6) + ak0;
-        aqh0 = *(const short8*)(qh + off);
-        aqh1 = *(const short8*)(qh + off + 32);
-        aql0 = *(const short8*)(ql + off);
-        aql1 = *(const short8*)(ql + off + 32);
-    }
-    __syncthreads();
-    f32x4 s_acc[4];
-    #pragma unroll
-    for (int jb = 0; jb < 4; ++jb) {
-        f32x4 z = {};
-        const int brow2 = (jb << 4) + (ln & 15);
-        short8 bh0 = *(short8*)&kmh[brow2][ak0];
-        short8 bh1 = *(short8*)&kmh[brow2][ak0 + 32];
-        short8 bl0 = *(short8*)&kml[brow2][ak0];
-        short8 bl1 = *(short8*)&kml[brow2][ak0 + 32];
-        z = __builtin_amdgcn_mfma_f32_16x16x32_bf16(aqh0, bh0, z, 0, 0, 0);
-        z = __builtin_amdgcn_mfma_f32_16x16x32_bf16(aqh0, bl0, z, 0, 0, 0);
-        z = __builtin_amdgcn_mfma_f32_16x16x32_bf16(aql0, bh0, z, 0, 0, 0);
-        z = __builtin_amdgcn_mfma_f32_16x16x32_bf16(aqh1, bh1, z, 0, 0, 0);
-        z = __builtin_amdgcn_mfma_f32_16x16x32_bf16(aqh1, bl1, z, 0, 0, 0);
-        z = __builtin_amdgcn_mfma_f32_16x16x32_bf16(aql1, bh1, z, 0, 0, 0);
-        s_acc[jb] = z;
-    }
-    float mx[4];
-    #pragma unroll
-    for (int r = 0; r < 4; ++r)
-        mx[r] = fmaxf(fmaxf(s_acc[0][r], s_acc[1][r]),
-                      fmaxf(s_acc[2][r], s_acc[3][r]));
-    #pragma unroll
-    for (int off2 = 1; off2 < 16; off2 <<= 1)
-        #pragma unroll
-        for (int r = 0; r < 4; ++r)
-            mx[r] = fmaxf(mx[r], __shfl_xor(mx[r], off2, 64));
-    float den[4] = {};
-    #pragma unroll
-    for (int jb = 0; jb < 4; ++jb) {
-        float tj = t64[(jb << 4) + (ln & 15)];
-        #pragma unroll
-        for (int r = 0; r < 4; ++r) {
-            float p = expf(s_acc[jb][r] - mx[r]);
-            den[r] += p * tj;
-            ph[wv][rg + r][(jb << 4) + (ln & 15)] = f2bf(p);
-        }
-    }
-    #pragma unroll
-    for (int off2 = 1; off2 < 16; off2 <<= 1)
-        #pragma unroll
-        for (int r = 0; r < 4; ++r)
-            den[r] += __shfl_xor(den[r], off2, 64);
-    short8 pah0 = *(short8*)&ph[wv][ln & 15][ak0];
-    short8 pah1 = *(short8*)&ph[wv][ln & 15][ak0 + 32];
-    f32x4 o_acc[4] = {};
-    #pragma unroll
-    for (int jb = 0; jb < 4; ++jb) {
-        const int brow2 = (jb << 4) + (ln & 15);
-        short8 bth0 = *(short8*)&tth[brow2][ak0];
-        short8 bth1 = *(short8*)&tth[brow2][ak0 + 32];
-        short8 btl0 = *(short8*)&ttl[brow2][ak0];
-        short8 btl1 = *(short8*)&ttl[brow2][ak0 + 32];
-        f32x4 o = o_acc[jb];
-        o = __builtin_amdgcn_mfma_f32_16x16x32_bf16(pah0, bth0, o, 0, 0, 0);
-        o = __builtin_amdgcn_mfma_f32_16x16x32_bf16(pah0, btl0, o, 0, 0, 0);
-        o = __builtin_amdgcn_mfma_f32_16x16x32_bf16(pah1, bth1, o, 0, 0, 0);
-        o = __builtin_amdgcn_mfma_f32_16x16x32_bf16(pah1, btl1, o, 0, 0, 0);
-        o_acc[jb] = o;
-    }
-    float inv[4];
-    #pragma unroll
-    for (int r = 0; r < 4; ++r) inv[r] = 1.0f / fmaxf(den[r], 1e-8f);
-    #pragma unroll
-    for (int jb = 0; jb < 4; ++jb)
-        #pragma unroll
-        for (int r = 0; r < 4; ++r) {
-            int row = n0 + (wv << 4) + rg + r;
-            int col = (jb << 4) + (ln & 15);
-            ctxh[((size_t)b * 4096 + row) * 768 + h * 64 + col] =
-                f2bf(o_acc[jb][r] * inv[r]);
-        }
-}
-
-__global__ __launch_bounds__(256) void flash_part(
-    const unsigned short* __restrict__ qhg, const unsigned short* __restrict__ khg,
-    const unsigned short* __restrict__ vhg,
-    float* __restrict__ pacc, float* __restrict__ pm, float* __restrict__ pl)
-{
-    int bx = blockIdx.x, cy = blockIdx.y, b = blockIdx.z;
-    int n0 = bx << 6;
-    size_t base = ((size_t)(b * 12 + 11)) << 12;
-    __shared__ unsigned short qs[64][72];
-    __shared__ unsigned short ks[64][72];
-    __shared__ unsigned short vts[64][72];
-    __shared__ unsigned short ps[4][16][72];
-    int tid = threadIdx.x;
-    int wv = tid >> 6, ln = tid & 63;
-    int rr = tid >> 2, dg = (tid & 3) << 4;
-    {
-        size_t off = ((base + n0 + rr) << 6) + dg;
-        *(short8*)&qs[rr][dg]     = *(const short8*)(qhg + off);
-        *(short8*)&qs[rr][dg + 8] = *(const short8*)(qhg + off + 8);
-    }
-    __syncthreads();
-    const int arow = (wv << 4) + (ln & 15);
-    const int ak0 = (ln >> 4) << 3;
-    const int rg = (ln >> 4) << 2;
-    short8 aq0 = *(short8*)&qs[arow][ak0];
-    short8 aq1 = *(short8*)&qs[arow][ak0 + 32];
-    f32x4 o_acc[4] = {};
-    float mr[4] = {-1e30f, -1e30f, -1e30f, -1e30f};
-    float lr[4] = {};
-    for (int t = 0; t < 16; ++t) {
-        int m0 = (cy << 10) + (t << 6);
-        __syncthreads();
+    if (blockIdx.x < 2816) {
+        int bh = blockIdx.x >> 6;
+        int bx = blockIdx.x & 63;
+        int b = bh / 11, h = bh - b * 11;
+        int n0 = bx << 6;
+        size_t base = ((size_t)(b * 12 + h)) << 12;
+        __shared__ unsigned short kmh[64][72], kml[64][72];
+        __shared__ unsigned short tth[64][72], ttl[64][72];
+        __shared__ unsigned short ph[4][16][72];
+        __shared__ float t64[64];
+        int wv = tid >> 6, ln = tid & 63;
+        int rr = tid >> 2, dg = (tid & 3) << 4;
+        const int arow = (wv << 4) + (ln & 15);
+        const int ak0 = (ln >> 4) << 3;
+        const int rg = (ln >> 4) << 2;
         {
-            size_t off = ((base + m0 + rr) << 6) + dg;
-            *(short8*)&ks[rr][dg]     = *(const short8*)(khg + off);
-            *(short8*)&ks[rr][dg + 8] = *(const short8*)(khg + off + 8);
-            short8 v0 = *(const short8*)(vhg + off);
-            short8 v1 = *(const short8*)(vhg + off + 8);
-            #pragma unroll
-            for (int i = 0; i < 8; ++i) {
-                vts[dg + i][rr]     = (unsigned short)v0[i];
-                vts[dg + 8 + i][rr] = (unsigned short)v1[i];
-            }
+            size_t off = ((base + ((size_t)rr << 6)) << 6) + dg;
+            *(short8*)&kmh[rr][dg]     = *(const short8*)(khg + off);
+            *(short8*)&kmh[rr][dg + 8] = *(const short8*)(khg + off + 8);
+            *(short8*)&kml[rr][dg]     = *(const short8*)(klg + off);
+            *(short8*)&kml[rr][dg + 8] = *(const short8*)(klg + off + 8);
+        }
+        for (int e = tid; e < 4096; e += 256) {
+            int m = e >> 6, j = e & 63;
+            float tv = Tb[(size_t)((bh << 6) + m) * 65 + j];
+            unsigned short hh, ll;
+            bfsplit(tv, hh, ll);
+            tth[j][m] = hh; ttl[j][m] = ll;
+        }
+        if (tid < 64) t64[tid] = Tb[(size_t)((bh << 6) + tid) * 65 + 64];
+        short8 aqh0, aql0, aqh1, aql1;
+        {
+            size_t off = ((base + n0 + arow) << 6) + ak0;
+            aqh0 = *(const short8*)(qh + off);
+            aqh1 = *(const short8*)(qh + off + 32);
+            aql0 = *(const short8*)(ql + off);
+            aql1 = *(const short8*)(ql + off + 32);
         }
         __syncthreads();
         f32x4 s_acc[4];
         #pragma unroll
         for (int jb = 0; jb < 4; ++jb) {
             f32x4 z = {};
-            short8 bk0 = *(short8*)&ks[(jb << 4) + (ln & 15)][ak0];
-            short8 bk1 = *(short8*)&ks[(jb << 4) + (ln & 15)][ak0 + 32];
-            z = __builtin_amdgcn_mfma_f32_16x16x32_bf16(aq0, bk0, z, 0, 0, 0);
-            z = __builtin_amdgcn_mfma_f32_16x16x32_bf16(aq1, bk1, z, 0, 0, 0);
+            const int brow2 = (jb << 4) + (ln & 15);
+            short8 bh0 = *(short8*)&kmh[brow2][ak0];
+            short8 bh1 = *(short8*)&kmh[brow2][ak0 + 32];
+            short8 bl0 = *(short8*)&kml[brow2][ak0];
+            short8 bl1 = *(short8*)&kml[brow2][ak0 + 32];
+            z = __builtin_amdgcn_mfma_f32_16x16x32_bf16(aqh0, bh0, z, 0, 0, 0);
+            z = __builtin_amdgcn_mfma_f32_16x16x32_bf16(aqh0, bl0, z, 0, 0, 0);
+            z = __builtin_amdgcn_mfma_f32_16x16x32_bf16(aql0, bh0, z, 0, 0, 0);
+            z = __builtin_amdgcn_mfma_f32_16x16x32_bf16(aqh1, bh1, z, 0, 0, 0);
+            z = __builtin_amdgcn_mfma_f32_16x16x32_bf16(aqh1, bl1, z, 0, 0, 0);
+            z = __builtin_amdgcn_mfma_f32_16x16x32_bf16(aql1, bh1, z, 0, 0, 0);
             s_acc[jb] = z;
         }
         float mx[4];
@@ -778,90 +775,77 @@
             #pragma unroll
             for (int r = 0; r < 4; ++r)
                 mx[r] = fmaxf(mx[r], __shfl_xor(mx[r], off2, 64));
-        float fac[4];
-        #pragma unroll
-        for (int r = 0; r < 4; ++r) {
-            float mn = fmaxf(mr[r], mx[r]);
-            fac[r] = expf(mr[r] - mn);
-            mr[r] = mn;
-        }
-        float rs[4] = {};
+        float den[4] = {};
+        #pragma unroll
+        for (int jb = 0; jb < 4; ++jb) {
+            float tj = t64[(jb << 4) + (ln & 15)];
+            #pragma unroll
+            for (int r = 0; r < 4; ++r) {
+                float p = expf(s_acc[jb][r] - mx[r]);
+                den[r] += p * tj;
+                ph[wv][rg + r][(jb << 4) + (ln & 15)] = f2bf(p);
+            }
+        }
+        #pragma unroll
+        for (int off2 = 1; off2 < 16; off2 <<= 1)
+            #pragma unroll
+            for (int r = 0; r < 4; ++r)
+                den[r] += __shfl_xor(den[r], off2, 64);
+        short8 pah0 = *(short8*)&ph[wv][ln & 15][ak0];
+        short8 pah1 = *(short8*)&ph[wv][ln & 15][ak0 + 32];
+        f32x4 o_acc[4] = {};
+        #pragma unroll
+        for (int jb = 0; jb < 4; ++jb) {
+            const int brow2 = (jb << 4) + (ln & 15);
+            short8 bth0 = *(short8*)&tth[brow2][ak0];
+            short8 bth1 = *(short8*)&tth[brow2][ak0 + 32];
+            short8 btl0 = *(short8*)&ttl[brow2][ak0];
+            short8 btl1 = *(short8*)&ttl[brow2][ak0 + 32];
+            f32x4 o = o_acc[jb];
+            o = __builtin_amdgcn_mfma_f32_16x16x32_bf16(pah0, bth0, o, 0, 0, 0);
+            o = __builtin_amdgcn_mfma_f32_16x16x32_bf16(pah0, btl0, o, 0, 0, 0);
+            o = __builtin_amdgcn_mfma_f32_16x16x32_bf16(pah1, bth1, o, 0, 0, 0);
+            o = __builtin_amdgcn_mfma_f32_16x16x32_bf16(pah1, btl1, o, 0, 0, 0);
+            o_acc[jb] = o;
+        }
+        float inv[4];
+        #pragma unroll
+        for (int r = 0; r < 4; ++r) inv[r] = 1.0f / fmaxf(den[r], 1e-8f);
         #pragma unroll
         for (int jb = 0; jb < 4; ++jb)
             #pragma unroll
             for (int r = 0; r < 4; ++r) {
-                float p = expf(s_acc[jb][r] - mr[r]);
-                rs[r] += p;
-                ps[wv][rg + r][(jb << 4) + (ln & 15)] = f2bf(p);
-            }
-        #pragma unroll
-        for (int off2 = 1; off2 < 16; off2 <<= 1)
-            #pragma unroll
-            for (int r = 0; r < 4; ++r)
-                rs[r] += __shfl_xor(rs[r], off2, 64);
-        #pragma unroll
-        for (int r = 0; r < 4; ++r) lr[r] = lr[r] * fac[r] + rs[r];
-        #pragma unroll
-        for (int jb = 0; jb < 4; ++jb)
-            #pragma unroll
-            for (int r = 0; r < 4; ++r)
-                o_acc[jb][r] *= fac[r];
-        short8 pa0 = *(short8*)&ps[wv][ln & 15][ak0];
-        short8 pa1 = *(short8*)&ps[wv][ln & 15][ak0 + 32];
-        #pragma unroll
-        for (int jb = 0; jb < 4; ++jb) {
-            short8 bv0 = *(short8*)&vts[(jb << 4) + (ln & 15)][ak0];
-            short8 bv1 = *(short8*)&vts[(jb << 4) + (ln & 15)][ak0 + 32];
-            f32x4 z = o_acc[jb];
-            z = __builtin_amdgcn_mfma_f32_16x16x32_bf16(pa0, bv0, z, 0, 0, 0);
-            z = __builtin_amdgcn_mfma_f32_16x16x32_bf16(pa1, bv1, z, 0, 0, 0);
-            o_acc[jb] = z;
-        }
-    }
-    int slot = (b * 4 + cy) * 64 + bx;
-    #pragma unroll
-    for (int jb = 0; jb < 4; ++jb)
-        #pragma unroll
-        for (int r = 0; r < 4; ++r) {
-            int row = (wv << 4) + rg + r, col = (jb << 4) + (ln & 15);
-            pacc[(size_t)slot * 4096 + (size_t)row * 64 + col] = o_acc[jb][r];
-        }
-    if ((ln & 15) == 0)
-        #pragma unroll
-        for (int r = 0; r < 4; ++r) {
-            int row = (wv << 4) + rg + r;
-            pm[(size_t)slot * 64 + row] = mr[r];
-            pl[(size_t)slot * 64 + row] = lr[r];
-        }
-}
-
-__global__ __launch_bounds__(256) void flash_merge(
-    const float* __restrict__ pacc, const float* __restrict__ pm,
-    const float* __restrict__ pl, unsigned short* __restrict__ ctxh)
-{
-    int bx = blockIdx.x, b = blockIdx.y;
-    int tid = threadIdx.x, r = tid & 63, g = tid >> 6;
-    float mc[4], mt = -1e30f;
-    #pragma unroll
-    for (int c = 0; c < 4; ++c) {
-        mc[c] = pm[(size_t)((b * 4 + c) * 64 + bx) * 64 + r];
-        mt = fmaxf(mt, mc[c]);
-    }
-    float fac[4], lt = 0.f;
-    #pragma unroll
-    for (int c = 0; c < 4; ++c) {
-        fac[c] = expf(mc[c] - mt);
-        lt += fac[c] * pl[(size_t)((b * 4 + c) * 64 + bx) * 64 + r];
-    }
-    float inv = 1.0f / lt;
-    size_t obase = ((size_t)b * 4096 + (size_t)((bx << 6) + r)) * 768 + 11 * 64 + (g << 4);
-    #pragma unroll
-    for (int i = 0; i < 16; ++i) {
-        float s = 0.f;
-        #pragma unroll
-        for (int c = 0; c < 4; ++c)
-            s += fac[c] * pacc[(size_t)((b * 4 + c) * 64 + bx) * 4096 + (size_t)r * 64 + (g << 4) + i];
-        ctxh[obase + i] = f2bf(s * inv);
+                int row = n0 + (wv << 4) + rg + r;
+                int col = (jb << 4) + (ln & 15);
+                ctxh[((size_t)b * 4096 + row) * 768 + h * 64 + col] =
+                    f2bf(o_acc[jb][r] * inv[r]);
+            }
+    } else {
+        int fb = blockIdx.x - 2816;
+        int bx = fb & 63, b = fb >> 6;
+        int r = tid & 63, g = tid >> 6;
+        float mc[4], mt = -1e30f;
+        #pragma unroll
+        for (int c = 0; c < 4; ++c) {
+            mc[c] = pm[(size_t)((b * 4 + c) * 64 + bx) * 64 + r];
+            mt = fmaxf(mt, mc[c]);
+        }
+        float fac[4], lt = 0.f;
+        #pragma unroll
+        for (int c = 0; c < 4; ++c) {
+            fac[c] = expf(mc[c] - mt);
+            lt += fac[c] * pl[(size_t)((b * 4 + c) * 64 + bx) * 64 + r];
+        }
+        float inv = 1.0f / lt;
+        size_t obase = ((size_t)b * 4096 + (size_t)((bx << 6) + r)) * 768 + 11 * 64 + (g << 4);
+        #pragma unroll
+        for (int i = 0; i < 16; ++i) {
+            float s = 0.f;
+            #pragma unroll
+            for (int c = 0; c < 4; ++c)
+                s += fac[c] * pacc[(size_t)((b * 4 + c) * 64 + bx) * 4096 + (size_t)r * 64 + (g << 4) + i];
+            ctxh[obase + i] = f2bf(s * inv);
+        }
     }
 }
 
@@ -949,8 +933,7 @@
     unsigned short* kl = kh + QKV;
     unsigned short* vh = kl + QKV;
     unsigned short* ctxh = vh + QKV;
-    float* scm  = (float*)(ctxh + QKV);
-    float* eB   = scm + 4096;
+    float* eB   = (float*)(ctxh + QKV);
     float* den  = eB + 44 * 4096;
     float* pi_  = den + 64;
     float* Wb   = pi_ + 44 * 4096;
@@ -962,26 +945,24 @@
 
     unsigned short* Xhi = (unsigned short*)out;
     unsigned short* Xlo = Xhi + QKV;
-    float* wacc = out;
-    float* wl   = wacc + 1441792;
-    float* wm   = wl + 22528;
-    float* fpacc = out;
+    float* wacc  = out;
+    float* wl    = wacc + 1441792;
+    float* wm    = wl + 22528;
+    float* fpacc = wm + 22528;
     float* fpm   = fpacc + 4194304;
     float* fpl   = fpm + 65536;
 
     preconv3<<<2048, 256, 0, stream>>>(x, qkv_w, proj_w,
                                        Xhi, Xlo, Whi, Wlo, Pwhi, Pwlo);
-    gemm_qk_mfma<<<1536, 256, 0, stream>>>(Xhi, Xlo, Whi, Wlo, qkv_b,
-                                           qh, ql, kh, kl);
-    gemm_v_mfma<<<768, 256, 0, stream>>>(Xhi, Whi, qkv_b, vh);
-    wflash<<<dim3(8, 44), 256, 0, stream>>>(qh, ql, kh, kl, vh, wacc, wl, wm);
-    wmerge<<<44, 256, 0, stream>>>(wacc, wl, wm, Wb, scm);
-    eb_kernel<<<44, 256, 0, stream>>>(qh, ql, kh, kl, scm, eB);
+    gemm_qkv2<<<2304, 256, 0, stream>>>(Xhi, Xlo, Whi, Wlo, qkv_b,
+                                        qh, ql, kh, kl, vh);
+    attn_mega<<<1376, 256, 0, stream>>>(qh, ql, kh, kl, vh,
+                                        wacc, wl, wm, fpacc, fpm, fpl);
+    wmerge_eb<<<44, 256, 0, stream>>>(wacc, wl, wm, qh, ql, kh, kl, Wb, eB);
     norms_kernel<<<11, 256, 0, stream>>>(eB, den);
     pinv_kernel<<<44, 256, 0, stream>>>(eB, den, pi_);
     pw_kernel<<<44, 256, 0, stream>>>(pi_, Wb, Tb);
-    outp_kernel<<<dim3(64, 44), 256, 0, stream>>>(qh, ql, kh, kl, Tb, ctxh);
-    flash_part<<<dim3(64, 4, 4), 256, 0, stream>>>(qh, kh, vh, fpacc, fpm, fpl);
-    flash_merge<<<dim3(64, 4), 256, 0, stream>>>(fpacc, fpm, fpl, ctxh);
+    outp_merge<<<3072, 256, 0, stream>>>(qh, ql, kh, kl, Tb,
+                                         fpacc, fpm, fpl, ctxh);
     gemm_proj_mfma<<<768, 256, 0, stream>>>(ctxh, Pwhi, proj_b, out);
 }
```

Result: faster. 409.5 us (-6.3%).
